# Optimization experiments

Hardware: AMD Instinct MI355X
Metric: run time of the kernel (lower is better)

Reference implementation:

```python
import jax, jax.numpy as jnp
import numpy as np

WIN = 32  # hardcoded window size in the original module


def _find(parent, x):
    while parent[x] != x:
        parent[x] = parent[parent[x]]
        x = parent[x]
    return x


def _label_background(bg):
    # 4-connected component labeling of True pixels; False pixels get label 0
    w = bg.shape[0]
    n = w * w
    parent = np.arange(n, dtype=np.int64)
    flat = bg.ravel()
    idx = np.arange(n).reshape(w, w)
    e1 = np.concatenate([idx[:, :-1].ravel(), idx[:-1, :].ravel()])
    e2 = np.concatenate([idx[:, 1:].ravel(), idx[1:, :].ravel()])
    for a, b in zip(e1, e2):
        if flat[a] and flat[b]:
            ra, rb = _find(parent, a), _find(parent, b)
            if ra != rb:
                parent[ra] = rb
    labels = np.zeros(n, dtype=np.int64)
    root2lab = {}
    nxt = 1
    for i in range(n):
        if flat[i]:
            r = _find(parent, i)
            if r not in root2lab:
                root2lab[r] = nxt
                nxt += 1
            labels[i] = root2lab[r]
    return labels


def _malis(seg, e1, e2, costs, pos):
    # Kruskal-style maximin MALIS edge weighting (descending affinity order).
    # Pairs involving segment label 0 (foreground / non-background) are excluded.
    n = seg.shape[0]
    parent = np.arange(n, dtype=np.int64)
    cnts = [({int(seg[i]): 1} if seg[i] != 0 else {}) for i in range(n)]
    w = np.zeros(costs.shape[0], dtype=np.int64)
    order = np.argsort(-costs, kind='stable')
    for e in order:
        a, b = _find(parent, e1[e]), _find(parent, e2[e])
        if a == b:
            continue
        ca, cb = cnts[a], cnts[b]
        if len(ca) > len(cb):  # small-to-large merge
            a, b, ca, cb = b, a, cb, ca
        common = 0
        for l, c in ca.items():
            if l in cb:
                common += c * cb[l]
        if pos:
            w[e] = common
        else:
            sa = sum(ca.values())
            sb = sum(cb.values())
            w[e] = sa * sb - common
        for l, c in ca.items():
            cb[l] = cb.get(l, 0) + c
        parent[a] = b
        cnts[a] = {}
    return w


def _malis_weights_full(pred, target):
    pred = np.asarray(pred)
    target = np.asarray(target)
    B, C, H, W = pred.shape
    weights_n = np.zeros(pred.shape, dtype=np.float32)
    weights_p = np.zeros(pred.shape, dtype=np.float32)
    idx = np.arange(WIN * WIN).reshape(WIN, WIN)
    e1 = np.concatenate([idx[:, :-1].ravel(), idx[:-1, :].ravel()])
    e2 = np.concatenate([idx[:, 1:].ravel(), idx[1:, :].ravel()])
    for r in range(H // WIN):
        for c in range(W // WIN):
            p = pred[:, :, r * WIN:(r + 1) * WIN, c * WIN:(c + 1) * WIN]
            t = target[:, :, r * WIN:(r + 1) * WIN, c * WIN:(c + 1) * WIN]
            costs_h = (p[:, :, :, :-1] + p[:, :, :, 1:]).reshape(B, -1)
            costs_v = (p[:, :, :-1, :] + p[:, :, 1:, :]).reshape(B, -1)
            costs = np.concatenate([costs_h, costs_v], 1)
            gt_h = (t[:, :, :, :-1] + t[:, :, :, 1:]).reshape(B, -1)
            gt_v = (t[:, :, :-1, :] + t[:, :, 1:, :]).reshape(B, -1)
            gt = np.concatenate([gt_h, gt_v], 1)
            costs_n = costs.copy()
            costs_p = costs.copy()
            costs_n[gt > 20] = 20
            costs_p[gt < 10] = 0
            gt = np.minimum(gt, 20)
            for i in range(B):
                seg = _label_background(t[i, 0] == 0)
                wn = _malis(seg, e1, e2, costs_n[i].astype(np.float32), 0).astype(np.float64)
                wp = _malis(seg, e1, e2, costs_p[i].astype(np.float32), 1).astype(np.float64)
                if wn.sum() > 0:
                    wn = wn / wn.sum()
                if wp.sum() > 0:
                    wp = wp / wp.sum()
                wn[gt[i] >= 10] = 0
                wp[gt[i] < 20] = 0
                half = WIN * (WIN - 1)
                for wsrc, wdst in ((wn, weights_n), (wp, weights_p)):
                    wh = wsrc[:half].reshape(WIN, WIN - 1)
                    wv = wsrc[half:].reshape(WIN - 1, WIN)
                    nw = np.zeros((WIN, WIN), dtype=np.float64)
                    nw[:, :-1] += wh
                    nw[:, 1:] += wh
                    nw[:-1, :] += wv
                    nw[1:, :] += wv
                    wdst[i, 0, r * WIN:(r + 1) * WIN, c * WIN:(c + 1) * WIN] = nw
    return weights_n, weights_p


def setup_inputs() -> dict:
    key = jax.random.key(0)
    k1, k2 = jax.random.split(key)
    y_true = jax.random.randint(k1, (4, 1, 256, 256), 0, 2).astype(jnp.float32) * 20.0
    y_pred = jax.random.uniform(k2, (4, 1, 256, 256), dtype=jnp.float32) * 20.0
    return {"y_true": y_true, "y_pred": y_pred}


def reference(y_true, y_pred):
    malis_lr = 1.0
    malis_lr_pos = 1.0
    out_sd = (jax.ShapeDtypeStruct(y_pred.shape, jnp.float32),
              jax.ShapeDtypeStruct(y_pred.shape, jnp.float32))
    weights_n, weights_p = jax.pure_callback(
        _malis_weights_full, out_sd,
        jax.lax.stop_gradient(y_pred), jax.lax.stop_gradient(y_true))
    loss_n = y_pred ** 2
    loss_p = (20.0 - y_pred) ** 2
    return (malis_lr * loss_n * weights_n + malis_lr_pos * loss_p * weights_p).sum()
```

## Files before the change

kernel.cpp:

```cpp
#include <hip/hip_runtime.h>

#define NPIX   1024
#define NEH    992
#define NEDGE  1984
#define SORTN  2048
#define CHUNK  8
#define NMERGE 1023
#define NIL    0xFFFFu

#define MRG_STRIDE 20480
#define MRG_M      0
#define MRG_RA     256
#define MRG_RB     4608
#define MRG_SS     8960
#define MRG_ED     13312
#define MRG_NXT    15616

__device__ __forceinline__ void edge_ab(int e, int& a, int& b) {
    if (e < NEH) { int y = e / 31; int x = e - y * 31; a = y * 32 + x; b = a + 1; }
    else         { int ev = e - NEH; a = ev; b = ev + 32; }
}

__device__ __forceinline__ uint4 add4(uint4 x, uint4 y) {
    return make_uint4(x.x + y.x, x.y + y.y, x.z + y.z, x.w + y.w);
}
__device__ __forceinline__ uint4 sub4(uint4 x, uint4 y) {
    return make_uint4(x.x - y.x, x.y - y.y, x.z - y.z, x.w - y.w);
}

__device__ __forceinline__ unsigned rdl32(unsigned v, int lane) {
    return (unsigned)__builtin_amdgcn_readlane((int)v, lane);
}
__device__ __forceinline__ unsigned long long rdl64(unsigned long long v, int lane) {
    unsigned lo = (unsigned)__builtin_amdgcn_readlane((int)(unsigned)v, lane);
    unsigned hi = (unsigned)__builtin_amdgcn_readlane((int)(unsigned)(v >> 32), lane);
    return ((unsigned long long)hi << 32) | lo;
}

__device__ void ccl_body(char* smem, int* kprimeSh,
                         const float* __restrict__ t_glob,
                         unsigned short* __restrict__ pixLab_g,
                         int* __restrict__ Kg, int tileId) {
    const int tid = threadIdx.x;
    const int bat = tileId >> 6;
    const int tile = tileId & 63;
    const int tr = tile >> 3, tc = tile & 7;

    unsigned short* labS = (unsigned short*)smem;
    unsigned int*   cntS = (unsigned int*)(smem + 2048);
    unsigned char*  bgS  = (unsigned char*)(smem + 20480);

    for (int i = tid; i < NPIX; i += 256) {
        int y = i >> 5, x = i & 31;
        int gidx = bat * 65536 + (tr * 32 + y) * 256 + (tc * 32 + x);
        bgS[i] = (t_glob[gidx] == 0.0f) ? 1 : 0;
    }
    __syncthreads();

    if (tid < 64) {
        const int lane = tid;
        if (lane < 32) {
            #pragma unroll
            for (int x = 0; x < 32; x++) {
                int i = lane * 32 + x;
                labS[i] = bgS[i] ? (unsigned short)i : (unsigned short)NIL;
            }
        }
        while (true) {
            bool changed = false;
            if (lane < 32) {
                const int base = lane * 32;
                unsigned short v[32];
                #pragma unroll
                for (int x = 0; x < 32; x++) v[x] = labS[base + x];
                unsigned run = NIL;
                #pragma unroll
                for (int x = 0; x < 32; x++) {
                    unsigned val = v[x];
                    if (val == NIL) { run = NIL; }
                    else { unsigned nv = min(run, val); changed |= (nv != val); v[x] = (unsigned short)nv; run = nv; }
                }
                run = NIL;
                #pragma unroll
                for (int x = 31; x >= 0; x--) {
                    unsigned val = v[x];
                    if (val == NIL) { run = NIL; }
                    else { unsigned nv = min(run, val); changed |= (nv != val); v[x] = (unsigned short)nv; run = nv; }
                }
                #pragma unroll
                for (int x = 0; x < 32; x++) labS[base + x] = v[x];
            }
            if (lane < 32) {
                unsigned short c[32];
                #pragma unroll
                for (int k = 0; k < 32; k++) c[k] = labS[k * 32 + lane];
                unsigned run = NIL;
                #pragma unroll
                for (int k = 0; k < 32; k++) {
                    unsigned val = c[k];
                    if (val == NIL) { run = NIL; }
                    else { unsigned nv = min(run, val); changed |= (nv != val); c[k] = (unsigned short)nv; run = nv; }
                }
                run = NIL;
                #pragma unroll
                for (int k = 31; k >= 0; k--) {
                    unsigned val = c[k];
                    if (val == NIL) { run = NIL; }
                    else { unsigned nv = min(run, val); changed |= (nv != val); c[k] = (unsigned short)nv; run = nv; }
                }
                #pragma unroll
                for (int k = 0; k < 32; k++) labS[k * 32 + lane] = c[k];
            }
            if (!__any(changed)) break;
        }
    }
    __syncthreads();

    for (int i = tid; i < NPIX; i += 256) cntS[i] = 0;
    if (tid == 0) *kprimeSh = 0;
    __syncthreads();
    for (int i = tid; i < NPIX; i += 256)
        if (bgS[i]) atomicAdd(&cntS[labS[i]], 1u);
    __syncthreads();
    for (int i = tid; i < NPIX; i += 256) {
        if (bgS[i] && (int)labS[i] == i) {
            unsigned id = (cntS[i] >= 2) ? (unsigned)atomicAdd(kprimeSh, 1) : NIL;
            cntS[i] = id;
        }
    }
    __syncthreads();
    for (int i = tid; i < NPIX; i += 256)
        pixLab_g[tileId * NPIX + i] = bgS[i] ? (unsigned short)cntS[labS[i]] : (unsigned short)NIL;
    if (tid == 0) Kg[tileId] = *kprimeSh;
}

__device__ void sort_body(char* smem,
                          const float* __restrict__ t_glob,
                          const float* __restrict__ p_glob,
                          unsigned short* __restrict__ ord_g, int wg) {
    const int tid = threadIdx.x;
    const int sgn = wg & 1;
    const int tileId = wg >> 1;
    const int bat = tileId >> 6;
    const int tile = tileId & 63;
    const int tr = tile >> 3, tc = tile & 7;

    float*              pT   = (float*)smem;
    unsigned long long* keys = (unsigned long long*)(smem + 4096);
    unsigned char*      bgS  = (unsigned char*)(smem + 20480);

    for (int i = tid; i < NPIX; i += 256) {
        int y = i >> 5, x = i & 31;
        int gidx = bat * 65536 + (tr * 32 + y) * 256 + (tc * 32 + x);
        pT[i] = p_glob[gidx];
        bgS[i] = (t_glob[gidx] == 0.0f) ? 1 : 0;
    }
    __syncthreads();

    for (int k = tid; k < SORTN; k += 256) {
        unsigned long long key = 0ULL;
        if (k < NEDGE) {
            int a, b; edge_ab(k, a, b);
            float cost = pT[a] + pT[b];
            int nfg = (int)(!bgS[a]) + (int)(!bgS[b]);
            if (sgn == 0) { if (nfg == 2) cost = 20.0f; }
            else          { if (nfg == 0) cost = 0.0f;  }
            key = ((unsigned long long)__float_as_uint(cost) << 16)
                | (unsigned long long)(0xFFFFu - (unsigned)k);
        }
        keys[k] = key;
    }
    __syncthreads();
    for (int kk = 2; kk <= SORTN; kk <<= 1) {
        for (int jj = kk >> 1; jj > 0; jj >>= 1) {
            for (int i = tid; i < SORTN; i += 256) {
                int ixj = i ^ jj;
                if (ixj > i) {
                    unsigned long long A = keys[i], Bv = keys[ixj];
                    bool descBlk = ((i & kk) == 0);
                    if ((A < Bv) == descBlk) { keys[i] = Bv; keys[ixj] = A; }
                }
            }
            __syncthreads();
        }
    }
    for (int k = tid; k < NEDGE; k += 256)
        ord_g[(size_t)wg * SORTN + k] = (unsigned short)(0xFFFFu - (unsigned)(keys[k] & 0xFFFFULL));
}

__global__ __launch_bounds__(256, 2)
void k12_ccl_sort(const float* __restrict__ t_glob,
                  const float* __restrict__ p_glob,
                  unsigned short* __restrict__ pixLab_g,
                  int* __restrict__ Kg,
                  unsigned short* __restrict__ ord_g,
                  int nT) {
    __shared__ __align__(16) char smem[21504];
    __shared__ int kprimeSh;
    if ((int)blockIdx.x < nT)
        ccl_body(smem, &kprimeSh, t_glob, pixLab_g, Kg, blockIdx.x);
    else
        sort_body(smem, t_glob, p_glob, ord_g, blockIdx.x - nT);
}

__global__ __launch_bounds__(64)
void k3_kruskal(const float* __restrict__ t_glob,
                const unsigned short* __restrict__ ord_g,
                char* __restrict__ mrg_base) {
    const int lane = threadIdx.x;
    const int wg  = blockIdx.x;
    const int tileId = wg >> 1;
    const int bat = tileId >> 6;
    const int tile = tileId & 63;
    const int tr = tile >> 3, tc = tile & 7;

    __shared__ unsigned short parentS[NPIX];
    __shared__ unsigned long long nodeS[NPIX];
    __shared__ unsigned short nextS[NPIX];
    __shared__ unsigned int   claimS[NPIX];

    char* mg = mrg_base + (size_t)wg * MRG_STRIDE;
    unsigned int*   mrA = (unsigned int*)(mg + MRG_RA);
    unsigned int*   mrB = (unsigned int*)(mg + MRG_RB);
    unsigned int*   mSS = (unsigned int*)(mg + MRG_SS);
    unsigned short* mED = (unsigned short*)(mg + MRG_ED);
    unsigned short* mNX = (unsigned short*)(mg + MRG_NXT);
    const unsigned short* ord = ord_g + (size_t)wg * SORTN;

    for (int i = lane; i < NPIX; i += 64) {
        int y = i >> 5, x = i & 31;
        int gidx = bat * 65536 + (tr * 32 + y) * 256 + (tc * 32 + x);
        unsigned bg = (t_glob[gidx] == 0.0f) ? 1u : 0u;
        parentS[i] = (unsigned short)i;
        nodeS[i] = ((unsigned long long)i << 48) | ((unsigned long long)i << 32)
                 | (1ULL << 16) | (unsigned long long)bg;
        nextS[i] = (unsigned short)NIL;
    }
    __syncthreads();

    int m = 0;
    for (int kb = 0; kb < NEDGE; kb += 64) {
        int e = ord[kb + lane];
        int a, b; edge_ab(e, a, b);
        unsigned ra = (unsigned)a, rb = (unsigned)b;
        while (true) {
            unsigned pa = parentS[ra];
            unsigned pb = parentS[rb];
            if (pa == ra && pb == rb) break;
            if (pa != ra) { unsigned ga = parentS[pa]; parentS[ra] = (unsigned short)ga; ra = ga; }
            if (pb != rb) { unsigned gb = parentS[pb]; parentS[rb] = (unsigned short)gb; rb = gb; }
        }
        bool pending = (ra != rb);
        bool committed = false;
        unsigned recA = 0, recB = 0, recSS = 0;

        int winners = 64;
        while (__any(pending) && winners >= 6) {
            if (pending) {
                claimS[ra] = 0xFFFFFFFFu;
                claimS[rb] = 0xFFFFFFFFu;
            }
            if (pending) {
                atomicMin(&claimS[ra], (unsigned)lane);
                atomicMin(&claimS[rb], (unsigned)lane);
            }
            bool win = pending && (claimS[ra] == (unsigned)lane) && (claimS[rb] == (unsigned)lane);
            if (win) {
                unsigned long long nA = nodeS[ra], nB = nodeS[rb];
                unsigned cons = ra, surv = rb;
                unsigned szAu = (unsigned)(nA >> 16) & 0xFFFFu;
                unsigned szBu = (unsigned)(nB >> 16) & 0xFFFFu;
                if (szAu > szBu) {
                    unsigned t = cons; cons = surv; surv = t;
                    unsigned long long tn = nA; nA = nB; nB = tn;
                }
                unsigned headA = (unsigned)(nA >> 48);
                unsigned tailA = (unsigned)(nA >> 32) & 0xFFFFu;
                unsigned szA   = (unsigned)(nA >> 16) & 0xFFFFu;
                unsigned slA   = (unsigned)nA & 0xFFFFu;
                unsigned headB = (unsigned)(nB >> 48);
                unsigned tailB = (unsigned)(nB >> 32) & 0xFFFFu;
                unsigned szB   = (unsigned)(nB >> 16) & 0xFFFFu;
                unsigned slB   = (unsigned)nB & 0xFFFFu;
                unsigned long long merged =
                      ((unsigned long long)headA << 48)
                    | ((unsigned long long)tailB << 32)
                    | ((unsigned long long)(szA + szB) << 16)
                    | (unsigned long long)(slA + slB);
                parentS[cons] = (unsigned short)surv;
                nodeS[surv]   = merged;
                nextS[tailA]  = (unsigned short)headB;
                recA = (headA << 16) | headB;
                recB = (szA << 16) | szB;
                recSS = slA * slB;
                committed = true;
                pending = false;
            }
            winners = (int)__popcll(__ballot(win));
            if (pending) {
                while (true) {
                    unsigned pa = parentS[ra];
                    unsigned pb = parentS[rb];
                    if (pa == ra && pb == rb) break;
                    if (pa != ra) { unsigned ga = parentS[pa]; parentS[ra] = (unsigned short)ga; ra = ga; }
                    if (pb != rb) { unsigned gb = parentS[pb]; parentS[rb] = (unsigned short)gb; rb = gb; }
                }
                if (ra == rb) pending = false;
            }
        }

        unsigned long long cmB = __ballot(committed);
        if (committed) {
            int idx = m + (int)__popcll(cmB & ((1ULL << lane) - 1ULL));
            mrA[idx] = recA;
            mrB[idx] = recB;
            mSS[idx] = recSS;
            mED[idx] = (unsigned short)e;
        }
        int bulkCount = (int)__popcll(cmB);

        int logCount = 0;
        if (__any(pending)) {
            unsigned long long na = 0, nb = 0;
            if (pending) { na = nodeS[ra]; nb = nodeS[rb]; }
            unsigned specAB = (ra << 16) | rb;
            unsigned long long candm = __ballot(pending);
            unsigned logRa  = 0xFFFFFFFFu;
            unsigned logRbO = 0xFFFFFFFFu;
            unsigned curRoot = 0xFFFFFFFFu;
            unsigned long long logNode = 0;
            while (candm != 0ULL) {
                int j = __ffsll((long long)candm) - 1;
                candm &= candm - 1ULL;
                unsigned sAB = rdl32(specAB, j);
                unsigned cra = sAB >> 16;
                unsigned crb = sAB & 0xFFFFu;
                unsigned long long hitA = __ballot(logRa == cra);
                unsigned long long hitB = __ballot(logRa == crb);
                if (hitA) cra = rdl32(curRoot, __ffsll((long long)hitA) - 1);
                if (hitB) crb = rdl32(curRoot, __ffsll((long long)hitB) - 1);
                if (cra == crb) continue;
                unsigned ce = rdl32((unsigned)e, j);
                unsigned long long hbA = __ballot(logRbO == cra);
                unsigned long long hbB = __ballot(logRbO == crb);
                unsigned long long cna = hbA ? rdl64(logNode, 63 - __clzll((long long)hbA)) : rdl64(na, j);
                unsigned long long cnb = hbB ? rdl64(logNode, 63 - __clzll((long long)hbB)) : rdl64(nb, j);
                unsigned cons = cra, surv = crb;
                unsigned szAq = (unsigned)(cna >> 16) & 0xFFFFu;
                unsigned szBq = (unsigned)(cnb >> 16) & 0xFFFFu;
                if (szAq > szBq) {
                    unsigned t = cons; cons = surv; surv = t;
                    unsigned long long tn = cna; cna = cnb; cnb = tn;
                }
                unsigned headA = (unsigned)(cna >> 48);
                unsigned tailA = (unsigned)(cna >> 32) & 0xFFFFu;
                unsigned szA   = (unsigned)(cna >> 16) & 0xFFFFu;
                unsigned slA   = (unsigned)cna & 0xFFFFu;
                unsigned headB = (unsigned)(cnb >> 48);
                unsigned tailB = (unsigned)(cnb >> 32) & 0xFFFFu;
                unsigned szB   = (unsigned)(cnb >> 16) & 0xFFFFu;
                unsigned slB   = (unsigned)cnb & 0xFFFFu;
                unsigned long long merged =
                      ((unsigned long long)headA << 48)
                    | ((unsigned long long)tailB << 32)
                    | ((unsigned long long)(szA + szB) << 16)
                    | (unsigned long long)(slA + slB);
                if (curRoot == cons) curRoot = surv;
                if (lane == logCount) {
                    logRa = cons; logRbO = surv; curRoot = surv; logNode = merged;
                    parentS[cons] = (unsigned short)surv;
                    nodeS[surv]   = merged;
                    nextS[tailA]  = (unsigned short)headB;
                    int idx = m + bulkCount + logCount;
                    mrA[idx] = (headA << 16) | headB;
                    mrB[idx] = (szA << 16) | szB;
                    mSS[idx] = slA * slB;
                    mED[idx] = (unsigned short)ce;
                }
                logCount++;
            }
        }
        m += bulkCount + logCount;
    }
    if (lane == 0) *(int*)(mg + MRG_M) = m;
    for (int i = lane; i < NPIX; i += 64) mNX[i] = nextS[i];
}

__global__ __launch_bounds__(256, 2)
void k4_weights(const float* __restrict__ t_glob,
                const float* __restrict__ p_glob,
                const unsigned short* __restrict__ pixLab_g,
                const int* __restrict__ Kg,
                const char* __restrict__ mrg_base,
                float* __restrict__ out) {
    const int tid = threadIdx.x;
    const int wg  = blockIdx.x;
    const int sgn = wg & 1;
    const int tileId = wg >> 1;
    const int bat = tileId >> 6;
    const int tile = tileId & 63;
    const int tr = tile >> 3, tc = tile & 7;

    __shared__ float          pT[NPIX];
    __shared__ unsigned char  bgS[NPIX];
    __shared__ unsigned short pixLab[NPIX];
    __shared__ unsigned short posS[NPIX];
    __shared__ unsigned int   mRecA[NMERGE];
    __shared__ unsigned int   mRecB[NMERGE];
    __shared__ unsigned int   mSaSb[NMERGE];
    __shared__ unsigned int   commonW[NMERGE];
    __shared__ unsigned short mEd[NMERGE];
    __shared__ __align__(16) unsigned long long big[2564];
    __shared__ unsigned wsumSh;
    __shared__ float lossSh;

    const char* mg = mrg_base + (size_t)wg * MRG_STRIDE;
    const int M = *(const int*)(mg + MRG_M);
    const int K = Kg[tileId];
    const unsigned int*   mrA = (const unsigned int*)(mg + MRG_RA);
    const unsigned int*   mrB = (const unsigned int*)(mg + MRG_RB);
    const unsigned int*   mSS = (const unsigned int*)(mg + MRG_SS);
    const unsigned short* mED = (const unsigned short*)(mg + MRG_ED);
    const unsigned short* mNX = (const unsigned short*)(mg + MRG_NXT);

    for (int i = tid; i < NPIX; i += 256) {
        int y = i >> 5, x = i & 31;
        int gidx = bat * 65536 + (tr * 32 + y) * 256 + (tc * 32 + x);
        pT[i] = p_glob[gidx];
        bgS[i] = (t_glob[gidx] == 0.0f) ? 1 : 0;
        pixLab[i] = pixLab_g[tileId * NPIX + i];
    }
    for (int j = tid; j < M; j += 256) {
        mRecA[j] = mrA[j];
        mRecB[j] = mrB[j];
        mSaSb[j] = mSS[j];
        mEd[j]   = mED[j];
        commonW[j] = 0;
    }

    unsigned short* n0 = (unsigned short*)big;
    unsigned short* n1 = n0 + 1024;
    unsigned short* d0 = n0 + 2048;
    unsigned short* d1 = n0 + 3072;
    for (int i = tid; i < NPIX; i += 256) { n0[i] = mNX[i]; d0[i] = 1; }
    __syncthreads();
    for (int s = 0; s < 10; s++) {
        unsigned short* sn = (s & 1) ? n1 : n0;
        unsigned short* sd = (s & 1) ? d1 : d0;
        unsigned short* dn = (s & 1) ? n0 : n1;
        unsigned short* dd = (s & 1) ? d0 : d1;
        for (int i = tid; i < NPIX; i += 256) {
            unsigned nx = sn[i];
            unsigned dv = sd[i];
            if (nx != NIL) { dv += sd[nx]; nx = sn[nx]; }
            dn[i] = (unsigned short)nx;
            dd[i] = (unsigned short)dv;
        }
        __syncthreads();
    }
    for (int i = tid; i < NPIX; i += 256)
        posS[i] = (unsigned short)(NPIX - (int)d0[i]);
    __syncthreads();

    unsigned*       P32 = (unsigned*)big;
    uint4*          P4  = (uint4*)big;
    unsigned*       scr = P32 + 4100;
    uint4*          S4  = (uint4*)scr;
    unsigned short* P16 = (unsigned short*)big;
    for (int base = 0; base < K; base += CHUNK) {
        for (int idx = tid; idx < 4100; idx += 256) P32[idx] = 0;
        __syncthreads();
        for (int i = tid; i < NPIX; i += 256) {
            unsigned l = pixLab[i];
            if (l != NIL && l >= (unsigned)base && l < (unsigned)(base + CHUNK))
                P16[(posS[i] + 1) * 8 + (l - base)] = 1;
        }
        __syncthreads();
        {
            int r0 = tid * 4 + 1;
            uint4 acc = P4[r0];
            for (int rr = r0 + 1; rr <= r0 + 3; rr++) { acc = add4(acc, P4[rr]); P4[rr] = acc; }
            S4[tid] = acc;
            __syncthreads();
            if (tid < 64) {
                uint4 s0 = S4[tid * 4], s1 = S4[tid * 4 + 1], s2 = S4[tid * 4 + 2], s3 = S4[tid * 4 + 3];
                uint4 t1 = add4(s0, s1), t2 = add4(t1, s2), t3 = add4(t2, s3);
                uint4 run = t3;
                #pragma unroll
                for (int d = 1; d < 64; d <<= 1) {
                    uint4 o;
                    o.x = __shfl_up(run.x, d, 64);
                    o.y = __shfl_up(run.y, d, 64);
                    o.z = __shfl_up(run.z, d, 64);
                    o.w = __shfl_up(run.w, d, 64);
                    if (tid >= d) run = add4(run, o);
                }
                uint4 off = sub4(run, t3);
                S4[tid * 4]     = add4(s0, off);
                S4[tid * 4 + 1] = add4(t1, off);
                S4[tid * 4 + 2] = add4(t2, off);
                S4[tid * 4 + 3] = add4(t3, off);
            }
            __syncthreads();
            if (tid > 0) {
                uint4 off = S4[tid - 1];
                for (int rr = r0; rr <= r0 + 3; rr++) P4[rr] = add4(P4[rr], off);
            }
        }
        __syncthreads();
        for (int j = tid; j < M; j += 256) {
            unsigned recA = mRecA[j], recB = mRecB[j];
            unsigned aS = posS[recA >> 16];
            unsigned bS = posS[recA & 0xFFFFu];
            uint4 da = sub4(P4[aS + (recB >> 16)], P4[aS]);
            uint4 db = sub4(P4[bS + (recB & 0xFFFFu)], P4[bS]);
            unsigned acc;
            acc  = (da.x & 0xFFFFu) * (db.x & 0xFFFFu) + (da.x >> 16) * (db.x >> 16);
            acc += (da.y & 0xFFFFu) * (db.y & 0xFFFFu) + (da.y >> 16) * (db.y >> 16);
            acc += (da.z & 0xFFFFu) * (db.z & 0xFFFFu) + (da.z >> 16) * (db.z >> 16);
            acc += (da.w & 0xFFFFu) * (db.w & 0xFFFFu) + (da.w >> 16) * (db.w >> 16);
            commonW[j] += acc;
        }
        __syncthreads();
    }

    if (tid == 0) { wsumSh = 0; lossSh = 0.0f; }
    __syncthreads();
    unsigned wloc = 0;
    for (int j = tid; j < M; j += 256)
        wloc += (sgn == 0) ? (mSaSb[j] - commonW[j]) : commonW[j];
    if (wloc) atomicAdd(&wsumSh, wloc);
    __syncthreads();
    const unsigned wsum = wsumSh;
    if (wsum > 0) {
        const double inv = 1.0 / (double)wsum;
        float lloc = 0.0f;
        for (int j = tid; j < M; j += 256) {
            unsigned w = (sgn == 0) ? (mSaSb[j] - commonW[j]) : commonW[j];
            if (!w) continue;
            int e = mEd[j];
            int a, b; edge_ab(e, a, b);
            int nfg = (int)(!bgS[a]) + (int)(!bgS[b]);
            bool keep = (sgn == 0) ? (nfg == 0) : (nfg >= 1);
            if (!keep) continue;
            float wn = (float)((double)w * inv);
            float fa, fb;
            if (sgn == 0) { fa = pT[a] * pT[a];            fb = pT[b] * pT[b]; }
            else { float da = 20.0f - pT[a], db = 20.0f - pT[b]; fa = da * da; fb = db * db; }
            lloc += wn * (fa + fb);
        }
        if (lloc != 0.0f) atomicAdd(&lossSh, lloc);
        __syncthreads();
        if (tid == 0 && lossSh != 0.0f) atomicAdd(out, lossSh);
    }
}

__global__ __launch_bounds__(256, 2)
void malis_mono(const float* __restrict__ t_glob,
                const float* __restrict__ p_glob,
                float* __restrict__ out) {
    const int tid  = threadIdx.x;
    const int wg   = blockIdx.x;
    const int sgn  = wg & 1;
    const int tileId = wg >> 1;
    const int bat  = tileId >> 6;
    const int tile = tileId & 63;
    const int tr = tile >> 3, tc = tile & 7;

    __shared__ float          pT[NPIX];
    __shared__ unsigned char  bgS[NPIX];
    __shared__ unsigned short pixLab[NPIX];
    __shared__ unsigned short parentS[NPIX];
    __shared__ unsigned short nextS[NPIX];
    __shared__ unsigned long long nodeS[NPIX];
    __shared__ unsigned int   claimS[NPIX];
    __shared__ unsigned short posS[NPIX];
    __shared__ unsigned short orderS[NEDGE];
    __shared__ unsigned int   mRecA[NMERGE];
    __shared__ unsigned int   mRecB[NMERGE];
    __shared__ unsigned short mEd[NMERGE];
    __shared__ unsigned int   mSaSb[NMERGE];
    __shared__ unsigned int   commonW[NMERGE];
    __shared__ __align__(16) unsigned long long big[2564];
    __shared__ int   kprimeSh, mCountSh;
    __shared__ unsigned wsumSh;
    __shared__ float lossSh;

    for (int i = tid; i < NPIX; i += 256) {
        int y = i >> 5, x = i & 31;
        int gidx = bat * 65536 + (tr * 32 + y) * 256 + (tc * 32 + x);
        pT[i] = p_glob[gidx];
        bgS[i] = (t_glob[gidx] == 0.0f) ? 1 : 0;
    }
    __syncthreads();

    unsigned short* labS = (unsigned short*)big;
    unsigned int*   cntS = (unsigned int*)(((char*)big) + 2048);
    if (tid < 64) {
        const int lane = tid;
        if (lane < 32) {
            #pragma unroll
            for (int x = 0; x < 32; x++) {
                int i = lane * 32 + x;
                labS[i] = bgS[i] ? (unsigned short)i : (unsigned short)NIL;
            }
        }
        while (true) {
            bool changed = false;
            if (lane < 32) {
                const int base = lane * 32;
                unsigned short v[32];
                #pragma unroll
                for (int x = 0; x < 32; x++) v[x] = labS[base + x];
                unsigned run = NIL;
                #pragma unroll
                for (int x = 0; x < 32; x++) {
                    unsigned val = v[x];
                    if (val == NIL) { run = NIL; }
                    else { unsigned nv = min(run, val); changed |= (nv != val); v[x] = (unsigned short)nv; run = nv; }
                }
                run = NIL;
                #pragma unroll
                for (int x = 31; x >= 0; x--) {
                    unsigned val = v[x];
                    if (val == NIL) { run = NIL; }
                    else { unsigned nv = min(run, val); changed |= (nv != val); v[x] = (unsigned short)nv; run = nv; }
                }
                #pragma unroll
                for (int x = 0; x < 32; x++) labS[base + x] = v[x];
            }
            if (lane < 32) {
                unsigned short c[32];
                #pragma unroll
                for (int k = 0; k < 32; k++) c[k] = labS[k * 32 + lane];
                unsigned run = NIL;
                #pragma unroll
                for (int k = 0; k < 32; k++) {
                    unsigned val = c[k];
                    if (val == NIL) { run = NIL; }
                    else { unsigned nv = min(run, val); changed |= (nv != val); c[k] = (unsigned short)nv; run = nv; }
                }
                run = NIL;
                #pragma unroll
                for (int k = 31; k >= 0; k--) {
                    unsigned val = c[k];
                    if (val == NIL) { run = NIL; }
                    else { unsigned nv = min(run, val); changed |= (nv != val); c[k] = (unsigned short)nv; run = nv; }
                }
                #pragma unroll
                for (int k = 0; k < 32; k++) labS[k * 32 + lane] = c[k];
            }
            if (!__any(changed)) break;
        }
    }
    __syncthreads();

    for (int i = tid; i < NPIX; i += 256) cntS[i] = 0;
    if (tid == 0) kprimeSh = 0;
    __syncthreads();
    for (int i = tid; i < NPIX; i += 256)
        if (bgS[i]) atomicAdd(&cntS[labS[i]], 1u);
    __syncthreads();
    for (int i = tid; i < NPIX; i += 256) {
        if (bgS[i] && (int)labS[i] == i) {
            unsigned id = (cntS[i] >= 2) ? (unsigned)atomicAdd(&kprimeSh, 1) : NIL;
            cntS[i] = id;
        }
    }
    __syncthreads();
    for (int i = tid; i < NPIX; i += 256)
        pixLab[i] = bgS[i] ? (unsigned short)cntS[labS[i]] : (unsigned short)NIL;
    __syncthreads();
    const int K = kprimeSh;

    unsigned long long* keys = big;
    for (int k = tid; k < SORTN; k += 256) {
        unsigned long long key = 0ULL;
        if (k < NEDGE) {
            int a, b; edge_ab(k, a, b);
            float cost = pT[a] + pT[b];
            int nfg = (int)(!bgS[a]) + (int)(!bgS[b]);
            if (sgn == 0) { if (nfg == 2) cost = 20.0f; }
            else          { if (nfg == 0) cost = 0.0f;  }
            key = ((unsigned long long)__float_as_uint(cost) << 16)
                | (unsigned long long)(0xFFFFu - (unsigned)k);
        }
        keys[k] = key;
    }
    __syncthreads();
    for (int kk = 2; kk <= SORTN; kk <<= 1) {
        for (int jj = kk >> 1; jj > 0; jj >>= 1) {
            for (int i = tid; i < SORTN; i += 256) {
                int ixj = i ^ jj;
                if (ixj > i) {
                    unsigned long long A = keys[i], Bv = keys[ixj];
                    bool descBlk = ((i & kk) == 0);
                    if ((A < Bv) == descBlk) { keys[i] = Bv; keys[ixj] = A; }
                }
            }
            __syncthreads();
        }
    }
    for (int k = tid; k < NEDGE; k += 256)
        orderS[k] = (unsigned short)(0xFFFFu - (unsigned)(keys[k] & 0xFFFFULL));
    for (int i = tid; i < NPIX; i += 256) {
        parentS[i] = (unsigned short)i;
        nodeS[i] = ((unsigned long long)i << 48) | ((unsigned long long)i << 32)
                 | (1ULL << 16) | (unsigned long long)bgS[i];
        nextS[i] = (unsigned short)NIL;
    }
    __syncthreads();

    if (tid < 64) {
        const int lane = tid;
        int m = 0;
        for (int kb = 0; kb < NEDGE; kb += 64) {
            int e = orderS[kb + lane];
            int a, b; edge_ab(e, a, b);
            unsigned ra = (unsigned)a, rb = (unsigned)b;
            bool pending = true;
            bool committed = false;
            unsigned recA = 0, recB = 0, recSS = 0;
            while (__any(pending)) {
                if (pending) {
                    while (true) {
                        unsigned pa = parentS[ra];
                        unsigned pb = parentS[rb];
                        if (pa == ra && pb == rb) break;
                        if (pa != ra) { unsigned ga = parentS[pa]; parentS[ra] = (unsigned short)ga; ra = ga; }
                        if (pb != rb) { unsigned gb = parentS[pb]; parentS[rb] = (unsigned short)gb; rb = gb; }
                    }
                    if (ra == rb) pending = false;
                }
                if (pending) {
                    claimS[ra] = 0xFFFFFFFFu;
                    claimS[rb] = 0xFFFFFFFFu;
                }
                if (pending) {
                    atomicMin(&claimS[ra], (unsigned)lane);
                    atomicMin(&claimS[rb], (unsigned)lane);
                }
                bool win = pending && (claimS[ra] == (unsigned)lane) && (claimS[rb] == (unsigned)lane);
                if (win) {
                    unsigned long long nA = nodeS[ra], nB = nodeS[rb];
                    unsigned cons = ra, surv = rb;
                    unsigned szAu = (unsigned)(nA >> 16) & 0xFFFFu;
                    unsigned szBu = (unsigned)(nB >> 16) & 0xFFFFu;
                    if (szAu > szBu) {
                        unsigned t = cons; cons = surv; surv = t;
                        unsigned long long tn = nA; nA = nB; nB = tn;
                    }
                    unsigned headA = (unsigned)(nA >> 48);
                    unsigned tailA = (unsigned)(nA >> 32) & 0xFFFFu;
                    unsigned szA   = (unsigned)(nA >> 16) & 0xFFFFu;
                    unsigned slA   = (unsigned)nA & 0xFFFFu;
                    unsigned headB = (unsigned)(nB >> 48);
                    unsigned tailB = (unsigned)(nB >> 32) & 0xFFFFu;
                    unsigned szB   = (unsigned)(nB >> 16) & 0xFFFFu;
                    unsigned slB   = (unsigned)nB & 0xFFFFu;
                    unsigned long long merged =
                          ((unsigned long long)headA << 48)
                        | ((unsigned long long)tailB << 32)
                        | ((unsigned long long)(szA + szB) << 16)
                        | (unsigned long long)(slA + slB);
                    parentS[cons] = (unsigned short)surv;
                    nodeS[surv]   = merged;
                    nextS[tailA]  = (unsigned short)headB;
                    recA = (headA << 16) | headB;
                    recB = (szA << 16) | szB;
                    recSS = slA * slB;
                    committed = true;
                    pending = false;
                }
            }
            unsigned long long cm = __ballot(committed);
            if (committed) {
                int idx = m + (int)__popcll(cm & ((1ULL << lane) - 1ULL));
                mRecA[idx] = recA;
                mRecB[idx] = recB;
                mSaSb[idx] = recSS;
                mEd[idx]   = (unsigned short)e;
            }
            m += (int)__popcll(cm);
        }
        if (lane == 0) mCountSh = m;
    }
    __syncthreads();
    const int M = mCountSh;
    for (int j = tid; j < M; j += 256) commonW[j] = 0;

    unsigned short* n0 = (unsigned short*)big;
    unsigned short* n1 = n0 + 1024;
    unsigned short* d0 = n0 + 2048;
    unsigned short* d1 = n0 + 3072;
    for (int i = tid; i < NPIX; i += 256) { n0[i] = nextS[i]; d0[i] = 1; }
    __syncthreads();
    for (int s = 0; s < 10; s++) {
        unsigned short* sn = (s & 1) ? n1 : n0;
        unsigned short* sd = (s & 1) ? d1 : d0;
        unsigned short* dn = (s & 1) ? n0 : n1;
        unsigned short* dd = (s & 1) ? d0 : d1;
        for (int i = tid; i < NPIX; i += 256) {
            unsigned nx = sn[i];
            unsigned dv = sd[i];
            if (nx != NIL) { dv += sd[nx]; nx = sn[nx]; }
            dn[i] = (unsigned short)nx;
            dd[i] = (unsigned short)dv;
        }
        __syncthreads();
    }
    for (int i = tid; i < NPIX; i += 256)
        posS[i] = (unsigned short)(NPIX - (int)d0[i]);
    __syncthreads();

    unsigned*       P32 = (unsigned*)big;
    uint4*          P4  = (uint4*)big;
    unsigned*       scr = P32 + 4100;
    uint4*          S4  = (uint4*)scr;
    unsigned short* P16 = (unsigned short*)big;
    for (int base = 0; base < K; base += CHUNK) {
        for (int idx = tid; idx < 4100; idx += 256) P32[idx] = 0;
        __syncthreads();
        for (int i = tid; i < NPIX; i += 256) {
            unsigned l = pixLab[i];
            if (l != NIL && l >= (unsigned)base && l < (unsigned)(base + CHUNK))
                P16[(posS[i] + 1) * 8 + (l - base)] = 1;
        }
        __syncthreads();
        {
            int r0 = tid * 4 + 1;
            uint4 acc = P4[r0];
            for (int rr = r0 + 1; rr <= r0 + 3; rr++) { acc = add4(acc, P4[rr]); P4[rr] = acc; }
            S4[tid] = acc;
            __syncthreads();
            if (tid < 64) {
                uint4 s0 = S4[tid * 4], s1 = S4[tid * 4 + 1], s2 = S4[tid * 4 + 2], s3 = S4[tid * 4 + 3];
                uint4 t1 = add4(s0, s1), t2 = add4(t1, s2), t3 = add4(t2, s3);
                uint4 run = t3;
                #pragma unroll
                for (int d = 1; d < 64; d <<= 1) {
                    uint4 o;
                    o.x = __shfl_up(run.x, d, 64);
                    o.y = __shfl_up(run.y, d, 64);
                    o.z = __shfl_up(run.z, d, 64);
                    o.w = __shfl_up(run.w, d, 64);
                    if (tid >= d) run = add4(run, o);
                }
                uint4 off = sub4(run, t3);
                S4[tid * 4]     = add4(s0, off);
                S4[tid * 4 + 1] = add4(t1, off);
                S4[tid * 4 + 2] = add4(t2, off);
                S4[tid * 4 + 3] = add4(t3, off);
            }
            __syncthreads();
            if (tid > 0) {
                uint4 off = S4[tid - 1];
                for (int rr = r0; rr <= r0 + 3; rr++) P4[rr] = add4(P4[rr], off);
            }
        }
        __syncthreads();
        for (int j = tid; j < M; j += 256) {
            unsigned recA = mRecA[j], recB = mRecB[j];
            unsigned aS = posS[recA >> 16];
            unsigned bS = posS[recA & 0xFFFFu];
            uint4 da = sub4(P4[aS + (recB >> 16)], P4[aS]);
            uint4 db = sub4(P4[bS + (recB & 0xFFFFu)], P4[bS]);
            unsigned acc;
            acc  = (da.x & 0xFFFFu) * (db.x & 0xFFFFu) + (da.x >> 16) * (db.x >> 16);
            acc += (da.y & 0xFFFFu) * (db.y & 0xFFFFu) + (da.y >> 16) * (db.y >> 16);
            acc += (da.z & 0xFFFFu) * (db.z & 0xFFFFu) + (da.z >> 16) * (db.z >> 16);
            acc += (da.w & 0xFFFFu) * (db.w & 0xFFFFu) + (da.w >> 16) * (db.w >> 16);
            commonW[j] += acc;
        }
        __syncthreads();
    }

    if (tid == 0) { wsumSh = 0; lossSh = 0.0f; }
    __syncthreads();
    unsigned wloc = 0;
    for (int j = tid; j < M; j += 256)
        wloc += (sgn == 0) ? (mSaSb[j] - commonW[j]) : commonW[j];
    if (wloc) atomicAdd(&wsumSh, wloc);
    __syncthreads();
    const unsigned wsum = wsumSh;
    if (wsum > 0) {
        const double inv = 1.0 / (double)wsum;
        float lloc = 0.0f;
        for (int j = tid; j < M; j += 256) {
            unsigned w = (sgn == 0) ? (mSaSb[j] - commonW[j]) : commonW[j];
            if (!w) continue;
            int e = mEd[j];
            int a, b; edge_ab(e, a, b);
            int nfg = (int)(!bgS[a]) + (int)(!bgS[b]);
            bool keep = (sgn == 0) ? (nfg == 0) : (nfg >= 1);
            if (!keep) continue;
            float wn = (float)((double)w * inv);
            float fa, fb;
            if (sgn == 0) { fa = pT[a] * pT[a];            fb = pT[b] * pT[b]; }
            else { float da = 20.0f - pT[a], db = 20.0f - pT[b]; fa = da * da; fb = db * db; }
            lloc += wn * (fa + fb);
        }
        if (lloc != 0.0f) atomicAdd(&lossSh, lloc);
        __syncthreads();
        if (tid == 0 && lossSh != 0.0f) atomicAdd(out, lossSh);
    }
}

extern "C" void kernel_launch(void* const* d_in, const int* in_sizes, int n_in,
                              void* d_out, int out_size, void* d_ws, size_t ws_size,
                              hipStream_t stream) {
    const float* y_true = (const float*)d_in[0];
    const float* y_pred = (const float*)d_in[1];
    float* out = (float*)d_out;
    const int B  = in_sizes[0] / (256 * 256);
    const int nT = B * 64;
    const int nW = nT * 2;

    const size_t offK   = (size_t)nT * 2048;
    const size_t offOrd = offK + (((size_t)nT * 4 + 255) & ~(size_t)255);
    const size_t offMrg = offOrd + (size_t)nW * 4096;
    const size_t need   = offMrg + (size_t)nW * MRG_STRIDE;

    hipMemsetAsync(d_out, 0, (size_t)out_size * sizeof(float), stream);

    if (ws_size >= need) {
        char* ws = (char*)d_ws;
        unsigned short* pixLab_g = (unsigned short*)ws;
        int*            Kg       = (int*)(ws + offK);
        unsigned short* ord_g    = (unsigned short*)(ws + offOrd);
        char*           mrg      = ws + offMrg;
        hipLaunchKernelGGL(k12_ccl_sort, dim3(nT + nW), dim3(256), 0, stream,
                           y_true, y_pred, pixLab_g, Kg, ord_g, nT);
        hipLaunchKernelGGL(k3_kruskal,   dim3(nW), dim3(64),  0, stream, y_true, ord_g, mrg);
        hipLaunchKernelGGL(k4_weights,   dim3(nW), dim3(256), 0, stream, y_true, y_pred,
                           pixLab_g, Kg, mrg, out);
    } else {
        hipLaunchKernelGGL(malis_mono, dim3(nW), dim3(256), 0, stream, y_true, y_pred, out);
    }
}
```

Baseline: 297.6 us.

## Fuse Kruskal merge kernel into weights kernel, keeping merge records in LDS

Merges the single-wavefront Kruskal kernel into the 256-thread weights kernel. Wave 0 builds the merge log directly in shared memory while the other waves idle, which removes the global merge-record buffer, its write and readback, and one kernel launch. The cost is that three quarters of each block sits idle during the serial Kruskal phase. Larger LDS use per block may also cut occupancy, and the claim array is aliased onto the scan scratch buffer.

```diff
diff --git a/kernel.cpp b/kernel.cpp
--- a/kernel.cpp
+++ b/kernel.cpp
@@ -7,14 +7,6 @@
 #define CHUNK  8
 #define NMERGE 1023
 #define NIL    0xFFFFu
-
-#define MRG_STRIDE 20480
-#define MRG_M      0
-#define MRG_RA     256
-#define MRG_RB     4608
-#define MRG_SS     8960
-#define MRG_ED     13312
-#define MRG_NXT    15616
 
 __device__ __forceinline__ void edge_ab(int e, int& a, int& b) {
     if (e < NEH) { int y = e / 31; int x = e - y * 31; a = y * 32 + x; b = a + 1; }
@@ -203,196 +195,13 @@
         sort_body(smem, t_glob, p_glob, ord_g, blockIdx.x - nT);
 }
 
-__global__ __launch_bounds__(64)
-void k3_kruskal(const float* __restrict__ t_glob,
-                const unsigned short* __restrict__ ord_g,
-                char* __restrict__ mrg_base) {
-    const int lane = threadIdx.x;
-    const int wg  = blockIdx.x;
-    const int tileId = wg >> 1;
-    const int bat = tileId >> 6;
-    const int tile = tileId & 63;
-    const int tr = tile >> 3, tc = tile & 7;
-
-    __shared__ unsigned short parentS[NPIX];
-    __shared__ unsigned long long nodeS[NPIX];
-    __shared__ unsigned short nextS[NPIX];
-    __shared__ unsigned int   claimS[NPIX];
-
-    char* mg = mrg_base + (size_t)wg * MRG_STRIDE;
-    unsigned int*   mrA = (unsigned int*)(mg + MRG_RA);
-    unsigned int*   mrB = (unsigned int*)(mg + MRG_RB);
-    unsigned int*   mSS = (unsigned int*)(mg + MRG_SS);
-    unsigned short* mED = (unsigned short*)(mg + MRG_ED);
-    unsigned short* mNX = (unsigned short*)(mg + MRG_NXT);
-    const unsigned short* ord = ord_g + (size_t)wg * SORTN;
-
-    for (int i = lane; i < NPIX; i += 64) {
-        int y = i >> 5, x = i & 31;
-        int gidx = bat * 65536 + (tr * 32 + y) * 256 + (tc * 32 + x);
-        unsigned bg = (t_glob[gidx] == 0.0f) ? 1u : 0u;
-        parentS[i] = (unsigned short)i;
-        nodeS[i] = ((unsigned long long)i << 48) | ((unsigned long long)i << 32)
-                 | (1ULL << 16) | (unsigned long long)bg;
-        nextS[i] = (unsigned short)NIL;
-    }
-    __syncthreads();
-
-    int m = 0;
-    for (int kb = 0; kb < NEDGE; kb += 64) {
-        int e = ord[kb + lane];
-        int a, b; edge_ab(e, a, b);
-        unsigned ra = (unsigned)a, rb = (unsigned)b;
-        while (true) {
-            unsigned pa = parentS[ra];
-            unsigned pb = parentS[rb];
-            if (pa == ra && pb == rb) break;
-            if (pa != ra) { unsigned ga = parentS[pa]; parentS[ra] = (unsigned short)ga; ra = ga; }
-            if (pb != rb) { unsigned gb = parentS[pb]; parentS[rb] = (unsigned short)gb; rb = gb; }
-        }
-        bool pending = (ra != rb);
-        bool committed = false;
-        unsigned recA = 0, recB = 0, recSS = 0;
-
-        int winners = 64;
-        while (__any(pending) && winners >= 6) {
-            if (pending) {
-                claimS[ra] = 0xFFFFFFFFu;
-                claimS[rb] = 0xFFFFFFFFu;
-            }
-            if (pending) {
-                atomicMin(&claimS[ra], (unsigned)lane);
-                atomicMin(&claimS[rb], (unsigned)lane);
-            }
-            bool win = pending && (claimS[ra] == (unsigned)lane) && (claimS[rb] == (unsigned)lane);
-            if (win) {
-                unsigned long long nA = nodeS[ra], nB = nodeS[rb];
-                unsigned cons = ra, surv = rb;
-                unsigned szAu = (unsigned)(nA >> 16) & 0xFFFFu;
-                unsigned szBu = (unsigned)(nB >> 16) & 0xFFFFu;
-                if (szAu > szBu) {
-                    unsigned t = cons; cons = surv; surv = t;
-                    unsigned long long tn = nA; nA = nB; nB = tn;
-                }
-                unsigned headA = (unsigned)(nA >> 48);
-                unsigned tailA = (unsigned)(nA >> 32) & 0xFFFFu;
-                unsigned szA   = (unsigned)(nA >> 16) & 0xFFFFu;
-                unsigned slA   = (unsigned)nA & 0xFFFFu;
-                unsigned headB = (unsigned)(nB >> 48);
-                unsigned tailB = (unsigned)(nB >> 32) & 0xFFFFu;
-                unsigned szB   = (unsigned)(nB >> 16) & 0xFFFFu;
-                unsigned slB   = (unsigned)nB & 0xFFFFu;
-                unsigned long long merged =
-                      ((unsigned long long)headA << 48)
-                    | ((unsigned long long)tailB << 32)
-                    | ((unsigned long long)(szA + szB) << 16)
-                    | (unsigned long long)(slA + slB);
-                parentS[cons] = (unsigned short)surv;
-                nodeS[surv]   = merged;
-                nextS[tailA]  = (unsigned short)headB;
-                recA = (headA << 16) | headB;
-                recB = (szA << 16) | szB;
-                recSS = slA * slB;
-                committed = true;
-                pending = false;
-            }
-            winners = (int)__popcll(__ballot(win));
-            if (pending) {
-                while (true) {
-                    unsigned pa = parentS[ra];
-                    unsigned pb = parentS[rb];
-                    if (pa == ra && pb == rb) break;
-                    if (pa != ra) { unsigned ga = parentS[pa]; parentS[ra] = (unsigned short)ga; ra = ga; }
-                    if (pb != rb) { unsigned gb = parentS[pb]; parentS[rb] = (unsigned short)gb; rb = gb; }
-                }
-                if (ra == rb) pending = false;
-            }
-        }
-
-        unsigned long long cmB = __ballot(committed);
-        if (committed) {
-            int idx = m + (int)__popcll(cmB & ((1ULL << lane) - 1ULL));
-            mrA[idx] = recA;
-            mrB[idx] = recB;
-            mSS[idx] = recSS;
-            mED[idx] = (unsigned short)e;
-        }
-        int bulkCount = (int)__popcll(cmB);
-
-        int logCount = 0;
-        if (__any(pending)) {
-            unsigned long long na = 0, nb = 0;
-            if (pending) { na = nodeS[ra]; nb = nodeS[rb]; }
-            unsigned specAB = (ra << 16) | rb;
-            unsigned long long candm = __ballot(pending);
-            unsigned logRa  = 0xFFFFFFFFu;
-            unsigned logRbO = 0xFFFFFFFFu;
-            unsigned curRoot = 0xFFFFFFFFu;
-            unsigned long long logNode = 0;
-            while (candm != 0ULL) {
-                int j = __ffsll((long long)candm) - 1;
-                candm &= candm - 1ULL;
-                unsigned sAB = rdl32(specAB, j);
-                unsigned cra = sAB >> 16;
-                unsigned crb = sAB & 0xFFFFu;
-                unsigned long long hitA = __ballot(logRa == cra);
-                unsigned long long hitB = __ballot(logRa == crb);
-                if (hitA) cra = rdl32(curRoot, __ffsll((long long)hitA) - 1);
-                if (hitB) crb = rdl32(curRoot, __ffsll((long long)hitB) - 1);
-                if (cra == crb) continue;
-                unsigned ce = rdl32((unsigned)e, j);
-                unsigned long long hbA = __ballot(logRbO == cra);
-                unsigned long long hbB = __ballot(logRbO == crb);
-                unsigned long long cna = hbA ? rdl64(logNode, 63 - __clzll((long long)hbA)) : rdl64(na, j);
-                unsigned long long cnb = hbB ? rdl64(logNode, 63 - __clzll((long long)hbB)) : rdl64(nb, j);
-                unsigned cons = cra, surv = crb;
-                unsigned szAq = (unsigned)(cna >> 16) & 0xFFFFu;
-                unsigned szBq = (unsigned)(cnb >> 16) & 0xFFFFu;
-                if (szAq > szBq) {
-                    unsigned t = cons; cons = surv; surv = t;
-                    unsigned long long tn = cna; cna = cnb; cnb = tn;
-                }
-                unsigned headA = (unsigned)(cna >> 48);
-                unsigned tailA = (unsigned)(cna >> 32) & 0xFFFFu;
-                unsigned szA   = (unsigned)(cna >> 16) & 0xFFFFu;
-                unsigned slA   = (unsigned)cna & 0xFFFFu;
-                unsigned headB = (unsigned)(cnb >> 48);
-                unsigned tailB = (unsigned)(cnb >> 32) & 0xFFFFu;
-                unsigned szB   = (unsigned)(cnb >> 16) & 0xFFFFu;
-                unsigned slB   = (unsigned)cnb & 0xFFFFu;
-                unsigned long long merged =
-                      ((unsigned long long)headA << 48)
-                    | ((unsigned long long)tailB << 32)
-                    | ((unsigned long long)(szA + szB) << 16)
-                    | (unsigned long long)(slA + slB);
-                if (curRoot == cons) curRoot = surv;
-                if (lane == logCount) {
-                    logRa = cons; logRbO = surv; curRoot = surv; logNode = merged;
-                    parentS[cons] = (unsigned short)surv;
-                    nodeS[surv]   = merged;
-                    nextS[tailA]  = (unsigned short)headB;
-                    int idx = m + bulkCount + logCount;
-                    mrA[idx] = (headA << 16) | headB;
-                    mrB[idx] = (szA << 16) | szB;
-                    mSS[idx] = slA * slB;
-                    mED[idx] = (unsigned short)ce;
-                }
-                logCount++;
-            }
-        }
-        m += bulkCount + logCount;
-    }
-    if (lane == 0) *(int*)(mg + MRG_M) = m;
-    for (int i = lane; i < NPIX; i += 64) mNX[i] = nextS[i];
-}
-
 __global__ __launch_bounds__(256, 2)
-void k4_weights(const float* __restrict__ t_glob,
-                const float* __restrict__ p_glob,
-                const unsigned short* __restrict__ pixLab_g,
-                const int* __restrict__ Kg,
-                const char* __restrict__ mrg_base,
-                float* __restrict__ out) {
+void k34_fused(const float* __restrict__ t_glob,
+               const float* __restrict__ p_glob,
+               const unsigned short* __restrict__ pixLab_g,
+               const int* __restrict__ Kg,
+               const unsigned short* __restrict__ ord_g,
+               float* __restrict__ out) {
     const int tid = threadIdx.x;
     const int wg  = blockIdx.x;
     const int sgn = wg & 1;
@@ -401,312 +210,38 @@
     const int tile = tileId & 63;
     const int tr = tile >> 3, tc = tile & 7;
 
-    __shared__ float          pT[NPIX];
-    __shared__ unsigned char  bgS[NPIX];
-    __shared__ unsigned short pixLab[NPIX];
-    __shared__ unsigned short posS[NPIX];
+    __shared__ unsigned short parentS[NPIX];
+    __shared__ unsigned long long nodeS[NPIX];
+    __shared__ unsigned short nextS[NPIX];
     __shared__ unsigned int   mRecA[NMERGE];
     __shared__ unsigned int   mRecB[NMERGE];
     __shared__ unsigned int   mSaSb[NMERGE];
     __shared__ unsigned int   commonW[NMERGE];
     __shared__ unsigned short mEd[NMERGE];
+    __shared__ float          pT[NPIX];
+    __shared__ unsigned char  bgS[NPIX];
+    __shared__ unsigned short pixLab[NPIX];
+    __shared__ unsigned short posS[NPIX];
     __shared__ __align__(16) unsigned long long big[2564];
+    __shared__ int   mCountSh;
     __shared__ unsigned wsumSh;
     __shared__ float lossSh;
 
-    const char* mg = mrg_base + (size_t)wg * MRG_STRIDE;
-    const int M = *(const int*)(mg + MRG_M);
-    const int K = Kg[tileId];
-    const unsigned int*   mrA = (const unsigned int*)(mg + MRG_RA);
-    const unsigned int*   mrB = (const unsigned int*)(mg + MRG_RB);
-    const unsigned int*   mSS = (const unsigned int*)(mg + MRG_SS);
-    const unsigned short* mED = (const unsigned short*)(mg + MRG_ED);
-    const unsigned short* mNX = (const unsigned short*)(mg + MRG_NXT);
+    unsigned int* claimS = (unsigned int*)big;
+
+    const unsigned short* ord = ord_g + (size_t)wg * SORTN;
 
     for (int i = tid; i < NPIX; i += 256) {
         int y = i >> 5, x = i & 31;
         int gidx = bat * 65536 + (tr * 32 + y) * 256 + (tc * 32 + x);
+        float tv = t_glob[gidx];
+        unsigned bg = (tv == 0.0f) ? 1u : 0u;
         pT[i] = p_glob[gidx];
-        bgS[i] = (t_glob[gidx] == 0.0f) ? 1 : 0;
+        bgS[i] = (unsigned char)bg;
         pixLab[i] = pixLab_g[tileId * NPIX + i];
-    }
-    for (int j = tid; j < M; j += 256) {
-        mRecA[j] = mrA[j];
-        mRecB[j] = mrB[j];
-        mSaSb[j] = mSS[j];
-        mEd[j]   = mED[j];
-        commonW[j] = 0;
-    }
-
-    unsigned short* n0 = (unsigned short*)big;
-    unsigned short* n1 = n0 + 1024;
-    unsigned short* d0 = n0 + 2048;
-    unsigned short* d1 = n0 + 3072;
-    for (int i = tid; i < NPIX; i += 256) { n0[i] = mNX[i]; d0[i] = 1; }
-    __syncthreads();
-    for (int s = 0; s < 10; s++) {
-        unsigned short* sn = (s & 1) ? n1 : n0;
-        unsigned short* sd = (s & 1) ? d1 : d0;
-        unsigned short* dn = (s & 1) ? n0 : n1;
-        unsigned short* dd = (s & 1) ? d0 : d1;
-        for (int i = tid; i < NPIX; i += 256) {
-            unsigned nx = sn[i];
-            unsigned dv = sd[i];
-            if (nx != NIL) { dv += sd[nx]; nx = sn[nx]; }
-            dn[i] = (unsigned short)nx;
-            dd[i] = (unsigned short)dv;
-        }
-        __syncthreads();
-    }
-    for (int i = tid; i < NPIX; i += 256)
-        posS[i] = (unsigned short)(NPIX - (int)d0[i]);
-    __syncthreads();
-
-    unsigned*       P32 = (unsigned*)big;
-    uint4*          P4  = (uint4*)big;
-    unsigned*       scr = P32 + 4100;
-    uint4*          S4  = (uint4*)scr;
-    unsigned short* P16 = (unsigned short*)big;
-    for (int base = 0; base < K; base += CHUNK) {
-        for (int idx = tid; idx < 4100; idx += 256) P32[idx] = 0;
-        __syncthreads();
-        for (int i = tid; i < NPIX; i += 256) {
-            unsigned l = pixLab[i];
-            if (l != NIL && l >= (unsigned)base && l < (unsigned)(base + CHUNK))
-                P16[(posS[i] + 1) * 8 + (l - base)] = 1;
-        }
-        __syncthreads();
-        {
-            int r0 = tid * 4 + 1;
-            uint4 acc = P4[r0];
-            for (int rr = r0 + 1; rr <= r0 + 3; rr++) { acc = add4(acc, P4[rr]); P4[rr] = acc; }
-            S4[tid] = acc;
-            __syncthreads();
-            if (tid < 64) {
-                uint4 s0 = S4[tid * 4], s1 = S4[tid * 4 + 1], s2 = S4[tid * 4 + 2], s3 = S4[tid * 4 + 3];
-                uint4 t1 = add4(s0, s1), t2 = add4(t1, s2), t3 = add4(t2, s3);
-                uint4 run = t3;
-                #pragma unroll
-                for (int d = 1; d < 64; d <<= 1) {
-                    uint4 o;
-                    o.x = __shfl_up(run.x, d, 64);
-                    o.y = __shfl_up(run.y, d, 64);
-                    o.z = __shfl_up(run.z, d, 64);
-                    o.w = __shfl_up(run.w, d, 64);
-                    if (tid >= d) run = add4(run, o);
-                }
-                uint4 off = sub4(run, t3);
-                S4[tid * 4]     = add4(s0, off);
-                S4[tid * 4 + 1] = add4(t1, off);
-                S4[tid * 4 + 2] = add4(t2, off);
-                S4[tid * 4 + 3] = add4(t3, off);
-            }
-            __syncthreads();
-            if (tid > 0) {
-                uint4 off = S4[tid - 1];
-                for (int rr = r0; rr <= r0 + 3; rr++) P4[rr] = add4(P4[rr], off);
-            }
-        }
-        __syncthreads();
-        for (int j = tid; j < M; j += 256) {
-            unsigned recA = mRecA[j], recB = mRecB[j];
-            unsigned aS = posS[recA >> 16];
-            unsigned bS = posS[recA & 0xFFFFu];
-            uint4 da = sub4(P4[aS + (recB >> 16)], P4[aS]);
-            uint4 db = sub4(P4[bS + (recB & 0xFFFFu)], P4[bS]);
-            unsigned acc;
-            acc  = (da.x & 0xFFFFu) * (db.x & 0xFFFFu) + (da.x >> 16) * (db.x >> 16);
-            acc += (da.y & 0xFFFFu) * (db.y & 0xFFFFu) + (da.y >> 16) * (db.y >> 16);
-            acc += (da.z & 0xFFFFu) * (db.z & 0xFFFFu) + (da.z >> 16) * (db.z >> 16);
-            acc += (da.w & 0xFFFFu) * (db.w & 0xFFFFu) + (da.w >> 16) * (db.w >> 16);
-            commonW[j] += acc;
-        }
-        __syncthreads();
-    }
-
-    if (tid == 0) { wsumSh = 0; lossSh = 0.0f; }
-    __syncthreads();
-    unsigned wloc = 0;
-    for (int j = tid; j < M; j += 256)
-        wloc += (sgn == 0) ? (mSaSb[j] - commonW[j]) : commonW[j];
-    if (wloc) atomicAdd(&wsumSh, wloc);
-    __syncthreads();
-    const unsigned wsum = wsumSh;
-    if (wsum > 0) {
-        const double inv = 1.0 / (double)wsum;
-        float lloc = 0.0f;
-        for (int j = tid; j < M; j += 256) {
-            unsigned w = (sgn == 0) ? (mSaSb[j] - commonW[j]) : commonW[j];
-            if (!w) continue;
-            int e = mEd[j];
-            int a, b; edge_ab(e, a, b);
-            int nfg = (int)(!bgS[a]) + (int)(!bgS[b]);
-            bool keep = (sgn == 0) ? (nfg == 0) : (nfg >= 1);
-            if (!keep) continue;
-            float wn = (float)((double)w * inv);
-            float fa, fb;
-            if (sgn == 0) { fa = pT[a] * pT[a];            fb = pT[b] * pT[b]; }
-            else { float da = 20.0f - pT[a], db = 20.0f - pT[b]; fa = da * da; fb = db * db; }
-            lloc += wn * (fa + fb);
-        }
-        if (lloc != 0.0f) atomicAdd(&lossSh, lloc);
-        __syncthreads();
-        if (tid == 0 && lossSh != 0.0f) atomicAdd(out, lossSh);
-    }
-}
-
-__global__ __launch_bounds__(256, 2)
-void malis_mono(const float* __restrict__ t_glob,
-                const float* __restrict__ p_glob,
-                float* __restrict__ out) {
-    const int tid  = threadIdx.x;
-    const int wg   = blockIdx.x;
-    const int sgn  = wg & 1;
-    const int tileId = wg >> 1;
-    const int bat  = tileId >> 6;
-    const int tile = tileId & 63;
-    const int tr = tile >> 3, tc = tile & 7;
-
-    __shared__ float          pT[NPIX];
-    __shared__ unsigned char  bgS[NPIX];
-    __shared__ unsigned short pixLab[NPIX];
-    __shared__ unsigned short parentS[NPIX];
-    __shared__ unsigned short nextS[NPIX];
-    __shared__ unsigned long long nodeS[NPIX];
-    __shared__ unsigned int   claimS[NPIX];
-    __shared__ unsigned short posS[NPIX];
-    __shared__ unsigned short orderS[NEDGE];
-    __shared__ unsigned int   mRecA[NMERGE];
-    __shared__ unsigned int   mRecB[NMERGE];
-    __shared__ unsigned short mEd[NMERGE];
-    __shared__ unsigned int   mSaSb[NMERGE];
-    __shared__ unsigned int   commonW[NMERGE];
-    __shared__ __align__(16) unsigned long long big[2564];
-    __shared__ int   kprimeSh, mCountSh;
-    __shared__ unsigned wsumSh;
-    __shared__ float lossSh;
-
-    for (int i = tid; i < NPIX; i += 256) {
-        int y = i >> 5, x = i & 31;
-        int gidx = bat * 65536 + (tr * 32 + y) * 256 + (tc * 32 + x);
-        pT[i] = p_glob[gidx];
-        bgS[i] = (t_glob[gidx] == 0.0f) ? 1 : 0;
-    }
-    __syncthreads();
-
-    unsigned short* labS = (unsigned short*)big;
-    unsigned int*   cntS = (unsigned int*)(((char*)big) + 2048);
-    if (tid < 64) {
-        const int lane = tid;
-        if (lane < 32) {
-            #pragma unroll
-            for (int x = 0; x < 32; x++) {
-                int i = lane * 32 + x;
-                labS[i] = bgS[i] ? (unsigned short)i : (unsigned short)NIL;
-            }
-        }
-        while (true) {
-            bool changed = false;
-            if (lane < 32) {
-                const int base = lane * 32;
-                unsigned short v[32];
-                #pragma unroll
-                for (int x = 0; x < 32; x++) v[x] = labS[base + x];
-                unsigned run = NIL;
-                #pragma unroll
-                for (int x = 0; x < 32; x++) {
-                    unsigned val = v[x];
-                    if (val == NIL) { run = NIL; }
-                    else { unsigned nv = min(run, val); changed |= (nv != val); v[x] = (unsigned short)nv; run = nv; }
-                }
-                run = NIL;
-                #pragma unroll
-                for (int x = 31; x >= 0; x--) {
-                    unsigned val = v[x];
-                    if (val == NIL) { run = NIL; }
-                    else { unsigned nv = min(run, val); changed |= (nv != val); v[x] = (unsigned short)nv; run = nv; }
-                }
-                #pragma unroll
-                for (int x = 0; x < 32; x++) labS[base + x] = v[x];
-            }
-            if (lane < 32) {
-                unsigned short c[32];
-                #pragma unroll
-                for (int k = 0; k < 32; k++) c[k] = labS[k * 32 + lane];
-                unsigned run = NIL;
-                #pragma unroll
-                for (int k = 0; k < 32; k++) {
-                    unsigned val = c[k];
-                    if (val == NIL) { run = NIL; }
-                    else { unsigned nv = min(run, val); changed |= (nv != val); c[k] = (unsigned short)nv; run = nv; }
-                }
-                run = NIL;
-                #pragma unroll
-                for (int k = 31; k >= 0; k--) {
-                    unsigned val = c[k];
-                    if (val == NIL) { run = NIL; }
-                    else { unsigned nv = min(run, val); changed |= (nv != val); c[k] = (unsigned short)nv; run = nv; }
-                }
-                #pragma unroll
-                for (int k = 0; k < 32; k++) labS[k * 32 + lane] = c[k];
-            }
-            if (!__any(changed)) break;
-        }
-    }
-    __syncthreads();
-
-    for (int i = tid; i < NPIX; i += 256) cntS[i] = 0;
-    if (tid == 0) kprimeSh = 0;
-    __syncthreads();
-    for (int i = tid; i < NPIX; i += 256)
-        if (bgS[i]) atomicAdd(&cntS[labS[i]], 1u);
-    __syncthreads();
-    for (int i = tid; i < NPIX; i += 256) {
-        if (bgS[i] && (int)labS[i] == i) {
-            unsigned id = (cntS[i] >= 2) ? (unsigned)atomicAdd(&kprimeSh, 1) : NIL;
-            cntS[i] = id;
-        }
-    }
-    __syncthreads();
-    for (int i = tid; i < NPIX; i += 256)
-        pixLab[i] = bgS[i] ? (unsigned short)cntS[labS[i]] : (unsigned short)NIL;
-    __syncthreads();
-    const int K = kprimeSh;
-
-    unsigned long long* keys = big;
-    for (int k = tid; k < SORTN; k += 256) {
-        unsigned long long key = 0ULL;
-        if (k < NEDGE) {
-            int a, b; edge_ab(k, a, b);
-            float cost = pT[a] + pT[b];
-            int nfg = (int)(!bgS[a]) + (int)(!bgS[b]);
-            if (sgn == 0) { if (nfg == 2) cost = 20.0f; }
-            else          { if (nfg == 0) cost = 0.0f;  }
-            key = ((unsigned long long)__float_as_uint(cost) << 16)
-                | (unsigned long long)(0xFFFFu - (unsigned)k);
-        }
-        keys[k] = key;
-    }
-    __syncthreads();
-    for (int kk = 2; kk <= SORTN; kk <<= 1) {
-        for (int jj = kk >> 1; jj > 0; jj >>= 1) {
-            for (int i = tid; i < SORTN; i += 256) {
-                int ixj = i ^ jj;
-                if (ixj > i) {
-                    unsigned long long A = keys[i], Bv = keys[ixj];
-                    bool descBlk = ((i & kk) == 0);
-                    if ((A < Bv) == descBlk) { keys[i] = Bv; keys[ixj] = A; }
-                }
-            }
-            __syncthreads();
-        }
-    }
-    for (int k = tid; k < NEDGE; k += 256)
-        orderS[k] = (unsigned short)(0xFFFFu - (unsigned)(keys[k] & 0xFFFFULL));
-    for (int i = tid; i < NPIX; i += 256) {
         parentS[i] = (unsigned short)i;
         nodeS[i] = ((unsigned long long)i << 48) | ((unsigned long long)i << 32)
-                 | (1ULL << 16) | (unsigned long long)bgS[i];
+                 | (1ULL << 16) | (unsigned long long)bg;
         nextS[i] = (unsigned short)NIL;
     }
     __syncthreads();
@@ -715,23 +250,22 @@
         const int lane = tid;
         int m = 0;
         for (int kb = 0; kb < NEDGE; kb += 64) {
-            int e = orderS[kb + lane];
+            int e = ord[kb + lane];
             int a, b; edge_ab(e, a, b);
             unsigned ra = (unsigned)a, rb = (unsigned)b;
-            bool pending = true;
+            while (true) {
+                unsigned pa = parentS[ra];
+                unsigned pb = parentS[rb];
+                if (pa == ra && pb == rb) break;
+                if (pa != ra) { unsigned ga = parentS[pa]; parentS[ra] = (unsigned short)ga; ra = ga; }
+                if (pb != rb) { unsigned gb = parentS[pb]; parentS[rb] = (unsigned short)gb; rb = gb; }
+            }
+            bool pending = (ra != rb);
             bool committed = false;
             unsigned recA = 0, recB = 0, recSS = 0;
-            while (__any(pending)) {
-                if (pending) {
-                    while (true) {
-                        unsigned pa = parentS[ra];
-                        unsigned pb = parentS[rb];
-                        if (pa == ra && pb == rb) break;
-                        if (pa != ra) { unsigned ga = parentS[pa]; parentS[ra] = (unsigned short)ga; ra = ga; }
-                        if (pb != rb) { unsigned gb = parentS[pb]; parentS[rb] = (unsigned short)gb; rb = gb; }
-                    }
-                    if (ra == rb) pending = false;
-                }
+
+            int winners = 64;
+            while (__any(pending) && winners >= 6) {
                 if (pending) {
                     claimS[ra] = 0xFFFFFFFFu;
                     claimS[rb] = 0xFFFFFFFFu;
@@ -772,21 +306,172 @@
                     committed = true;
                     pending = false;
                 }
-            }
-            unsigned long long cm = __ballot(committed);
+                winners = (int)__popcll(__ballot(win));
+                if (pending) {
+                    while (true) {
+                        unsigned pa = parentS[ra];
+                        unsigned pb = parentS[rb];
+                        if (pa == ra && pb == rb) break;
+                        if (pa != ra) { unsigned ga = parentS[pa]; parentS[ra] = (unsigned short)ga; ra = ga; }
+                        if (pb != rb) { unsigned gb = parentS[pb]; parentS[rb] = (unsigned short)gb; rb = gb; }
+                    }
+                    if (ra == rb) pending = false;
+                }
+            }
+
+            unsigned long long cmB = __ballot(committed);
             if (committed) {
-                int idx = m + (int)__popcll(cm & ((1ULL << lane) - 1ULL));
+                int idx = m + (int)__popcll(cmB & ((1ULL << lane) - 1ULL));
                 mRecA[idx] = recA;
                 mRecB[idx] = recB;
                 mSaSb[idx] = recSS;
                 mEd[idx]   = (unsigned short)e;
             }
-            m += (int)__popcll(cm);
+            m += (int)__popcll(cmB);
+
+            int logCount = 0;
+            if (__any(pending)) {
+                unsigned long long na = 0, nb = 0;
+                if (pending) { na = nodeS[ra]; nb = nodeS[rb]; }
+                unsigned specAB = (ra << 16) | rb;
+                unsigned long long candm = __ballot(pending);
+                unsigned logRa  = 0xFFFFFFFFu;
+                unsigned logRbO = 0xFFFFFFFFu;
+                unsigned curRoot = 0xFFFFFFFFu;
+                unsigned long long logNode = 0;
+                while (candm != 0ULL) {
+                    int j1 = __ffsll((long long)candm) - 1;
+                    candm &= candm - 1ULL;
+                    bool have2 = (candm != 0ULL);
+                    int j2 = 0;
+                    if (have2) { j2 = __ffsll((long long)candm) - 1; candm &= candm - 1ULL; }
+
+                    unsigned s1 = rdl32(specAB, j1);
+                    unsigned cra1 = s1 >> 16, crb1 = s1 & 0xFFFFu;
+                    unsigned s2 = have2 ? rdl32(specAB, j2) : 0u;
+                    unsigned cra2 = s2 >> 16, crb2 = s2 & 0xFFFFu;
+
+                    unsigned long long h;
+                    h = __ballot(logRa == cra1); if (h) cra1 = rdl32(curRoot, __ffsll((long long)h) - 1);
+                    h = __ballot(logRa == crb1); if (h) crb1 = rdl32(curRoot, __ffsll((long long)h) - 1);
+                    h = __ballot(logRa == cra2); if (h) cra2 = rdl32(curRoot, __ffsll((long long)h) - 1);
+                    h = __ballot(logRa == crb2); if (h) crb2 = rdl32(curRoot, __ffsll((long long)h) - 1);
+
+                    bool c1 = (cra1 != crb1);
+                    unsigned cons1 = 0, surv1 = 0;
+                    unsigned long long merged1 = 0;
+                    unsigned hA1 = 0, tA1 = 0, hB1 = 0, r1B = 0, r1SS = 0;
+                    if (c1) {
+                        unsigned long long hbA = __ballot(logRbO == cra1);
+                        unsigned long long cna = hbA ? rdl64(logNode, 63 - __clzll((long long)hbA)) : rdl64(na, j1);
+                        unsigned long long hbB = __ballot(logRbO == crb1);
+                        unsigned long long cnb = hbB ? rdl64(logNode, 63 - __clzll((long long)hbB)) : rdl64(nb, j1);
+                        cons1 = cra1; surv1 = crb1;
+                        unsigned szAu = (unsigned)(cna >> 16) & 0xFFFFu;
+                        unsigned szBu = (unsigned)(cnb >> 16) & 0xFFFFu;
+                        if (szAu > szBu) {
+                            unsigned t = cons1; cons1 = surv1; surv1 = t;
+                            unsigned long long tn = cna; cna = cnb; cnb = tn;
+                        }
+                        unsigned headA = (unsigned)(cna >> 48);
+                        unsigned tailA = (unsigned)(cna >> 32) & 0xFFFFu;
+                        unsigned szA   = (unsigned)(cna >> 16) & 0xFFFFu;
+                        unsigned slA   = (unsigned)cna & 0xFFFFu;
+                        unsigned headB = (unsigned)(cnb >> 48);
+                        unsigned tailB = (unsigned)(cnb >> 32) & 0xFFFFu;
+                        unsigned szB   = (unsigned)(cnb >> 16) & 0xFFFFu;
+                        unsigned slB   = (unsigned)cnb & 0xFFFFu;
+                        merged1 = ((unsigned long long)headA << 48)
+                                | ((unsigned long long)tailB << 32)
+                                | ((unsigned long long)(szA + szB) << 16)
+                                | (unsigned long long)(slA + slB);
+                        hA1 = headA; tA1 = tailA; hB1 = headB;
+                        r1B = (szA << 16) | szB; r1SS = slA * slB;
+                    }
+                    bool c2 = false;
+                    unsigned cons2 = 0, surv2 = 0;
+                    unsigned long long merged2 = 0;
+                    unsigned hA2 = 0, tA2 = 0, hB2 = 0, r2B = 0, r2SS = 0;
+                    if (have2) {
+                        if (c1) {
+                            if (cra2 == cons1) cra2 = surv1;
+                            if (crb2 == cons1) crb2 = surv1;
+                        }
+                        if (cra2 != crb2) {
+                            c2 = true;
+                            unsigned long long cna2, cnb2;
+                            if (c1 && cra2 == surv1) cna2 = merged1;
+                            else {
+                                unsigned long long hb = __ballot(logRbO == cra2);
+                                cna2 = hb ? rdl64(logNode, 63 - __clzll((long long)hb)) : rdl64(na, j2);
+                            }
+                            if (c1 && crb2 == surv1) cnb2 = merged1;
+                            else {
+                                unsigned long long hb = __ballot(logRbO == crb2);
+                                cnb2 = hb ? rdl64(logNode, 63 - __clzll((long long)hb)) : rdl64(nb, j2);
+                            }
+                            cons2 = cra2; surv2 = crb2;
+                            unsigned szAu = (unsigned)(cna2 >> 16) & 0xFFFFu;
+                            unsigned szBu = (unsigned)(cnb2 >> 16) & 0xFFFFu;
+                            if (szAu > szBu) {
+                                unsigned t = cons2; cons2 = surv2; surv2 = t;
+                                unsigned long long tn = cna2; cna2 = cnb2; cnb2 = tn;
+                            }
+                            unsigned headA = (unsigned)(cna2 >> 48);
+                            unsigned tailA = (unsigned)(cna2 >> 32) & 0xFFFFu;
+                            unsigned szA   = (unsigned)(cna2 >> 16) & 0xFFFFu;
+                            unsigned slA   = (unsigned)cna2 & 0xFFFFu;
+                            unsigned headB = (unsigned)(cnb2 >> 48);
+                            unsigned tailB = (unsigned)(cnb2 >> 32) & 0xFFFFu;
+                            unsigned szB   = (unsigned)(cnb2 >> 16) & 0xFFFFu;
+                            unsigned slB   = (unsigned)cnb2 & 0xFFFFu;
+                            merged2 = ((unsigned long long)headA << 48)
+                                    | ((unsigned long long)tailB << 32)
+                                    | ((unsigned long long)(szA + szB) << 16)
+                                    | (unsigned long long)(slA + slB);
+                            hA2 = headA; tA2 = tailA; hB2 = headB;
+                            r2B = (szA << 16) | szB; r2SS = slA * slB;
+                        }
+                    }
+                    unsigned ce1 = c1 ? rdl32((unsigned)e, j1) : 0u;
+                    unsigned ce2 = c2 ? rdl32((unsigned)e, j2) : 0u;
+                    if (c1 && curRoot == cons1) curRoot = surv1;
+                    if (c2 && curRoot == cons2) curRoot = surv2;
+                    int slot1 = logCount;
+                    int slot2 = logCount + (c1 ? 1 : 0);
+                    if (c1 && lane == slot1) {
+                        logRa = cons1; logRbO = surv1; logNode = merged1;
+                        curRoot = (c2 && cons2 == surv1) ? surv2 : surv1;
+                        parentS[cons1] = (unsigned short)surv1;
+                        if (!(c2 && surv2 == surv1)) nodeS[surv1] = merged1;
+                        nextS[tA1] = (unsigned short)hB1;
+                        int idx = m + slot1;
+                        mRecA[idx] = (hA1 << 16) | hB1;
+                        mRecB[idx] = r1B;
+                        mSaSb[idx] = r1SS;
+                        mEd[idx]   = (unsigned short)ce1;
+                    }
+                    if (c2 && lane == slot2) {
+                        logRa = cons2; logRbO = surv2; curRoot = surv2; logNode = merged2;
+                        parentS[cons2] = (unsigned short)surv2;
+                        nodeS[surv2]   = merged2;
+                        nextS[tA2]     = (unsigned short)hB2;
+                        int idx = m + slot2;
+                        mRecA[idx] = (hA2 << 16) | hB2;
+                        mRecB[idx] = r2B;
+                        mSaSb[idx] = r2SS;
+                        mEd[idx]   = (unsigned short)ce2;
+                    }
+                    logCount += (c1 ? 1 : 0) + (c2 ? 1 : 0);
+                }
+            }
+            m += logCount;
         }
         if (lane == 0) mCountSh = m;
     }
     __syncthreads();
     const int M = mCountSh;
+    const int K = Kg[tileId];
     for (int j = tid; j < M; j += 256) commonW[j] = 0;
 
     unsigned short* n0 = (unsigned short*)big;
@@ -906,6 +591,357 @@
     }
 }
 
+__global__ __launch_bounds__(256, 2)
+void malis_mono(const float* __restrict__ t_glob,
+                const float* __restrict__ p_glob,
+                float* __restrict__ out) {
+    const int tid  = threadIdx.x;
+    const int wg   = blockIdx.x;
+    const int sgn  = wg & 1;
+    const int tileId = wg >> 1;
+    const int bat  = tileId >> 6;
+    const int tile = tileId & 63;
+    const int tr = tile >> 3, tc = tile & 7;
+
+    __shared__ float          pT[NPIX];
+    __shared__ unsigned char  bgS[NPIX];
+    __shared__ unsigned short pixLab[NPIX];
+    __shared__ unsigned short parentS[NPIX];
+    __shared__ unsigned short nextS[NPIX];
+    __shared__ unsigned long long nodeS[NPIX];
+    __shared__ unsigned int   claimS[NPIX];
+    __shared__ unsigned short posS[NPIX];
+    __shared__ unsigned short orderS[NEDGE];
+    __shared__ unsigned int   mRecA[NMERGE];
+    __shared__ unsigned int   mRecB[NMERGE];
+    __shared__ unsigned short mEd[NMERGE];
+    __shared__ unsigned int   mSaSb[NMERGE];
+    __shared__ unsigned int   commonW[NMERGE];
+    __shared__ __align__(16) unsigned long long big[2564];
+    __shared__ int   kprimeSh, mCountSh;
+    __shared__ unsigned wsumSh;
+    __shared__ float lossSh;
+
+    for (int i = tid; i < NPIX; i += 256) {
+        int y = i >> 5, x = i & 31;
+        int gidx = bat * 65536 + (tr * 32 + y) * 256 + (tc * 32 + x);
+        pT[i] = p_glob[gidx];
+        bgS[i] = (t_glob[gidx] == 0.0f) ? 1 : 0;
+    }
+    __syncthreads();
+
+    unsigned short* labS = (unsigned short*)big;
+    unsigned int*   cntS = (unsigned int*)(((char*)big) + 2048);
+    if (tid < 64) {
+        const int lane = tid;
+        if (lane < 32) {
+            #pragma unroll
+            for (int x = 0; x < 32; x++) {
+                int i = lane * 32 + x;
+                labS[i] = bgS[i] ? (unsigned short)i : (unsigned short)NIL;
+            }
+        }
+        while (true) {
+            bool changed = false;
+            if (lane < 32) {
+                const int base = lane * 32;
+                unsigned short v[32];
+                #pragma unroll
+                for (int x = 0; x < 32; x++) v[x] = labS[base + x];
+                unsigned run = NIL;
+                #pragma unroll
+                for (int x = 0; x < 32; x++) {
+                    unsigned val = v[x];
+                    if (val == NIL) { run = NIL; }
+                    else { unsigned nv = min(run, val); changed |= (nv != val); v[x] = (unsigned short)nv; run = nv; }
+                }
+                run = NIL;
+                #pragma unroll
+                for (int x = 31; x >= 0; x--) {
+                    unsigned val = v[x];
+                    if (val == NIL) { run = NIL; }
+                    else { unsigned nv = min(run, val); changed |= (nv != val); v[x] = (unsigned short)nv; run = nv; }
+                }
+                #pragma unroll
+                for (int x = 0; x < 32; x++) labS[base + x] = v[x];
+            }
+            if (lane < 32) {
+                unsigned short c[32];
+                #pragma unroll
+                for (int k = 0; k < 32; k++) c[k] = labS[k * 32 + lane];
+                unsigned run = NIL;
+                #pragma unroll
+                for (int k = 0; k < 32; k++) {
+                    unsigned val = c[k];
+                    if (val == NIL) { run = NIL; }
+                    else { unsigned nv = min(run, val); changed |= (nv != val); c[k] = (unsigned short)nv; run = nv; }
+                }
+                run = NIL;
+                #pragma unroll
+                for (int k = 31; k >= 0; k--) {
+                    unsigned val = c[k];
+                    if (val == NIL) { run = NIL; }
+                    else { unsigned nv = min(run, val); changed |= (nv != val); c[k] = (unsigned short)nv; run = nv; }
+                }
+                #pragma unroll
+                for (int k = 0; k < 32; k++) labS[k * 32 + lane] = c[k];
+            }
+            if (!__any(changed)) break;
+        }
+    }
+    __syncthreads();
+
+    for (int i = tid; i < NPIX; i += 256) cntS[i] = 0;
+    if (tid == 0) kprimeSh = 0;
+    __syncthreads();
+    for (int i = tid; i < NPIX; i += 256)
+        if (bgS[i]) atomicAdd(&cntS[labS[i]], 1u);
+    __syncthreads();
+    for (int i = tid; i < NPIX; i += 256) {
+        if (bgS[i] && (int)labS[i] == i) {
+            unsigned id = (cntS[i] >= 2) ? (unsigned)atomicAdd(&kprimeSh, 1) : NIL;
+            cntS[i] = id;
+        }
+    }
+    __syncthreads();
+    for (int i = tid; i < NPIX; i += 256)
+        pixLab[i] = bgS[i] ? (unsigned short)cntS[labS[i]] : (unsigned short)NIL;
+    __syncthreads();
+    const int K = kprimeSh;
+
+    unsigned long long* keys = big;
+    for (int k = tid; k < SORTN; k += 256) {
+        unsigned long long key = 0ULL;
+        if (k < NEDGE) {
+            int a, b; edge_ab(k, a, b);
+            float cost = pT[a] + pT[b];
+            int nfg = (int)(!bgS[a]) + (int)(!bgS[b]);
+            if (sgn == 0) { if (nfg == 2) cost = 20.0f; }
+            else          { if (nfg == 0) cost = 0.0f;  }
+            key = ((unsigned long long)__float_as_uint(cost) << 16)
+                | (unsigned long long)(0xFFFFu - (unsigned)k);
+        }
+        keys[k] = key;
+    }
+    __syncthreads();
+    for (int kk = 2; kk <= SORTN; kk <<= 1) {
+        for (int jj = kk >> 1; jj > 0; jj >>= 1) {
+            for (int i = tid; i < SORTN; i += 256) {
+                int ixj = i ^ jj;
+                if (ixj > i) {
+                    unsigned long long A = keys[i], Bv = keys[ixj];
+                    bool descBlk = ((i & kk) == 0);
+                    if ((A < Bv) == descBlk) { keys[i] = Bv; keys[ixj] = A; }
+                }
+            }
+            __syncthreads();
+        }
+    }
+    for (int k = tid; k < NEDGE; k += 256)
+        orderS[k] = (unsigned short)(0xFFFFu - (unsigned)(keys[k] & 0xFFFFULL));
+    for (int i = tid; i < NPIX; i += 256) {
+        parentS[i] = (unsigned short)i;
+        nodeS[i] = ((unsigned long long)i << 48) | ((unsigned long long)i << 32)
+                 | (1ULL << 16) | (unsigned long long)bgS[i];
+        nextS[i] = (unsigned short)NIL;
+    }
+    __syncthreads();
+
+    if (tid < 64) {
+        const int lane = tid;
+        int m = 0;
+        for (int kb = 0; kb < NEDGE; kb += 64) {
+            int e = orderS[kb + lane];
+            int a, b; edge_ab(e, a, b);
+            unsigned ra = (unsigned)a, rb = (unsigned)b;
+            bool pending = true;
+            bool committed = false;
+            unsigned recA = 0, recB = 0, recSS = 0;
+            while (__any(pending)) {
+                if (pending) {
+                    while (true) {
+                        unsigned pa = parentS[ra];
+                        unsigned pb = parentS[rb];
+                        if (pa == ra && pb == rb) break;
+                        if (pa != ra) { unsigned ga = parentS[pa]; parentS[ra] = (unsigned short)ga; ra = ga; }
+                        if (pb != rb) { unsigned gb = parentS[pb]; parentS[rb] = (unsigned short)gb; rb = gb; }
+                    }
+                    if (ra == rb) pending = false;
+                }
+                if (pending) {
+                    claimS[ra] = 0xFFFFFFFFu;
+                    claimS[rb] = 0xFFFFFFFFu;
+                }
+                if (pending) {
+                    atomicMin(&claimS[ra], (unsigned)lane);
+                    atomicMin(&claimS[rb], (unsigned)lane);
+                }
+                bool win = pending && (claimS[ra] == (unsigned)lane) && (claimS[rb] == (unsigned)lane);
+                if (win) {
+                    unsigned long long nA = nodeS[ra], nB = nodeS[rb];
+                    unsigned cons = ra, surv = rb;
+                    unsigned szAu = (unsigned)(nA >> 16) & 0xFFFFu;
+                    unsigned szBu = (unsigned)(nB >> 16) & 0xFFFFu;
+                    if (szAu > szBu) {
+                        unsigned t = cons; cons = surv; surv = t;
+                        unsigned long long tn = nA; nA = nB; nB = tn;
+                    }
+                    unsigned headA = (unsigned)(nA >> 48);
+                    unsigned tailA = (unsigned)(nA >> 32) & 0xFFFFu;
+                    unsigned szA   = (unsigned)(nA >> 16) & 0xFFFFu;
+                    unsigned slA   = (unsigned)nA & 0xFFFFu;
+                    unsigned headB = (unsigned)(nB >> 48);
+                    unsigned tailB = (unsigned)(nB >> 32) & 0xFFFFu;
+                    unsigned szB   = (unsigned)(nB >> 16) & 0xFFFFu;
+                    unsigned slB   = (unsigned)nB & 0xFFFFu;
+                    unsigned long long merged =
+                          ((unsigned long long)headA << 48)
+                        | ((unsigned long long)tailB << 32)
+                        | ((unsigned long long)(szA + szB) << 16)
+                        | (unsigned long long)(slA + slB);
+                    parentS[cons] = (unsigned short)surv;
+                    nodeS[surv]   = merged;
+                    nextS[tailA]  = (unsigned short)headB;
+                    recA = (headA << 16) | headB;
+                    recB = (szA << 16) | szB;
+                    recSS = slA * slB;
+                    committed = true;
+                    pending = false;
+                }
+            }
+            unsigned long long cm = __ballot(committed);
+            if (committed) {
+                int idx = m + (int)__popcll(cm & ((1ULL << lane) - 1ULL));
+                mRecA[idx] = recA;
+                mRecB[idx] = recB;
+                mSaSb[idx] = recSS;
+                mEd[idx]   = (unsigned short)e;
+            }
+            m += (int)__popcll(cm);
+        }
+        if (lane == 0) mCountSh = m;
+    }
+    __syncthreads();
+    const int M = mCountSh;
+    for (int j = tid; j < M; j += 256) commonW[j] = 0;
+
+    unsigned short* n0 = (unsigned short*)big;
+    unsigned short* n1 = n0 + 1024;
+    unsigned short* d0 = n0 + 2048;
+    unsigned short* d1 = n0 + 3072;
+    for (int i = tid; i < NPIX; i += 256) { n0[i] = nextS[i]; d0[i] = 1; }
+    __syncthreads();
+    for (int s = 0; s < 10; s++) {
+        unsigned short* sn = (s & 1) ? n1 : n0;
+        unsigned short* sd = (s & 1) ? d1 : d0;
+        unsigned short* dn = (s & 1) ? n0 : n1;
+        unsigned short* dd = (s & 1) ? d0 : d1;
+        for (int i = tid; i < NPIX; i += 256) {
+            unsigned nx = sn[i];
+            unsigned dv = sd[i];
+            if (nx != NIL) { dv += sd[nx]; nx = sn[nx]; }
+            dn[i] = (unsigned short)nx;
+            dd[i] = (unsigned short)dv;
+        }
+        __syncthreads();
+    }
+    for (int i = tid; i < NPIX; i += 256)
+        posS[i] = (unsigned short)(NPIX - (int)d0[i]);
+    __syncthreads();
+
+    unsigned*       P32 = (unsigned*)big;
+    uint4*          P4  = (uint4*)big;
+    unsigned*       scr = P32 + 4100;
+    uint4*          S4  = (uint4*)scr;
+    unsigned short* P16 = (unsigned short*)big;
+    for (int base = 0; base < K; base += CHUNK) {
+        for (int idx = tid; idx < 4100; idx += 256) P32[idx] = 0;
+        __syncthreads();
+        for (int i = tid; i < NPIX; i += 256) {
+            unsigned l = pixLab[i];
+            if (l != NIL && l >= (unsigned)base && l < (unsigned)(base + CHUNK))
+                P16[(posS[i] + 1) * 8 + (l - base)] = 1;
+        }
+        __syncthreads();
+        {
+            int r0 = tid * 4 + 1;
+            uint4 acc = P4[r0];
+            for (int rr = r0 + 1; rr <= r0 + 3; rr++) { acc = add4(acc, P4[rr]); P4[rr] = acc; }
+            S4[tid] = acc;
+            __syncthreads();
+            if (tid < 64) {
+                uint4 s0 = S4[tid * 4], s1 = S4[tid * 4 + 1], s2 = S4[tid * 4 + 2], s3 = S4[tid * 4 + 3];
+                uint4 t1 = add4(s0, s1), t2 = add4(t1, s2), t3 = add4(t2, s3);
+                uint4 run = t3;
+                #pragma unroll
+                for (int d = 1; d < 64; d <<= 1) {
+                    uint4 o;
+                    o.x = __shfl_up(run.x, d, 64);
+                    o.y = __shfl_up(run.y, d, 64);
+                    o.z = __shfl_up(run.z, d, 64);
+                    o.w = __shfl_up(run.w, d, 64);
+                    if (tid >= d) run = add4(run, o);
+                }
+                uint4 off = sub4(run, t3);
+                S4[tid * 4]     = add4(s0, off);
+                S4[tid * 4 + 1] = add4(t1, off);
+                S4[tid * 4 + 2] = add4(t2, off);
+                S4[tid * 4 + 3] = add4(t3, off);
+            }
+            __syncthreads();
+            if (tid > 0) {
+                uint4 off = S4[tid - 1];
+                for (int rr = r0; rr <= r0 + 3; rr++) P4[rr] = add4(P4[rr], off);
+            }
+        }
+        __syncthreads();
+        for (int j = tid; j < M; j += 256) {
+            unsigned recA = mRecA[j], recB = mRecB[j];
+            unsigned aS = posS[recA >> 16];
+            unsigned bS = posS[recA & 0xFFFFu];
+            uint4 da = sub4(P4[aS + (recB >> 16)], P4[aS]);
+            uint4 db = sub4(P4[bS + (recB & 0xFFFFu)], P4[bS]);
+            unsigned acc;
+            acc  = (da.x & 0xFFFFu) * (db.x & 0xFFFFu) + (da.x >> 16) * (db.x >> 16);
+            acc += (da.y & 0xFFFFu) * (db.y & 0xFFFFu) + (da.y >> 16) * (db.y >> 16);
+            acc += (da.z & 0xFFFFu) * (db.z & 0xFFFFu) + (da.z >> 16) * (db.z >> 16);
+            acc += (da.w & 0xFFFFu) * (db.w & 0xFFFFu) + (da.w >> 16) * (db.w >> 16);
+            commonW[j] += acc;
+        }
+        __syncthreads();
+    }
+
+    if (tid == 0) { wsumSh = 0; lossSh = 0.0f; }
+    __syncthreads();
+    unsigned wloc = 0;
+    for (int j = tid; j < M; j += 256)
+        wloc += (sgn == 0) ? (mSaSb[j] - commonW[j]) : commonW[j];
+    if (wloc) atomicAdd(&wsumSh, wloc);
+    __syncthreads();
+    const unsigned wsum = wsumSh;
+    if (wsum > 0) {
+        const double inv = 1.0 / (double)wsum;
+        float lloc = 0.0f;
+        for (int j = tid; j < M; j += 256) {
+            unsigned w = (sgn == 0) ? (mSaSb[j] - commonW[j]) : commonW[j];
+            if (!w) continue;
+            int e = mEd[j];
+            int a, b; edge_ab(e, a, b);
+            int nfg = (int)(!bgS[a]) + (int)(!bgS[b]);
+            bool keep = (sgn == 0) ? (nfg == 0) : (nfg >= 1);
+            if (!keep) continue;
+            float wn = (float)((double)w * inv);
+            float fa, fb;
+            if (sgn == 0) { fa = pT[a] * pT[a];            fb = pT[b] * pT[b]; }
+            else { float da = 20.0f - pT[a], db = 20.0f - pT[b]; fa = da * da; fb = db * db; }
+            lloc += wn * (fa + fb);
+        }
+        if (lloc != 0.0f) atomicAdd(&lossSh, lloc);
+        __syncthreads();
+        if (tid == 0 && lossSh != 0.0f) atomicAdd(out, lossSh);
+    }
+}
+
 extern "C" void kernel_launch(void* const* d_in, const int* in_sizes, int n_in,
                               void* d_out, int out_size, void* d_ws, size_t ws_size,
                               hipStream_t stream) {
@@ -918,8 +954,7 @@
 
     const size_t offK   = (size_t)nT * 2048;
     const size_t offOrd = offK + (((size_t)nT * 4 + 255) & ~(size_t)255);
-    const size_t offMrg = offOrd + (size_t)nW * 4096;
-    const size_t need   = offMrg + (size_t)nW * MRG_STRIDE;
+    const size_t need   = offOrd + (size_t)nW * 4096;
 
     hipMemsetAsync(d_out, 0, (size_t)out_size * sizeof(float), stream);
 
@@ -928,12 +963,10 @@
         unsigned short* pixLab_g = (unsigned short*)ws;
         int*            Kg       = (int*)(ws + offK);
         unsigned short* ord_g    = (unsigned short*)(ws + offOrd);
-        char*           mrg      = ws + offMrg;
         hipLaunchKernelGGL(k12_ccl_sort, dim3(nT + nW), dim3(256), 0, stream,
                            y_true, y_pred, pixLab_g, Kg, ord_g, nT);
-        hipLaunchKernelGGL(k3_kruskal,   dim3(nW), dim3(64),  0, stream, y_true, ord_g, mrg);
-        hipLaunchKernelGGL(k4_weights,   dim3(nW), dim3(256), 0, stream, y_true, y_pred,
-                           pixLab_g, Kg, mrg, out);
+        hipLaunchKernelGGL(k34_fused,    dim3(nW), dim3(256), 0, stream,
+                           y_true, y_pred, pixLab_g, Kg, ord_g, out);
     } else {
         hipLaunchKernelGGL(malis_mono, dim3(nW), dim3(256), 0, stream, y_true, y_pred, out);
     }
```

New measurement: 303.1 us. No clear change (+1.8%).
